# Kernel tuning notes

Hardware: AMD Instinct MI355X
Metric: run time of the kernel (lower is better)

Reference implementation:

```python
import jax, jax.numpy as jnp
import numpy as np
import math
from jax import lax

IMG = 800.0
STRIDES = (8, 16, 32)
SIZES = (100, 50, 25)
PAD = 100
ANCHOR_SIZES = (32., 64., 128., 256., 512.)
RATIOS = (0.5, 1.0, 2.0)
A = 15
PRE_NMS = 500
POST_NMS = 512
RPN_NMS_THR = 0.7
BOX_NMS_THR = 0.5
SCORE_THR = 0.05
DETS = 100
POOL = 7
SR = 2
CH = 256
NUM_CLASSES = 2
CLIP = math.log(1000.0 / 16)


def _grid_anchors():
    scales = np.array(ANCHOR_SIZES, np.float32)
    hr = np.sqrt(np.array(RATIOS, np.float32)); wr = 1.0 / hr
    ws = (wr[:, None] * scales[None]).reshape(-1)
    hs = (hr[:, None] * scales[None]).reshape(-1)
    base = np.stack([-ws, -hs, ws, hs], 1) / 2.0
    out = []
    for stride, s in zip(STRIDES, SIZES):
        sx = np.arange(s, dtype=np.float32) * stride
        yy, xx = np.meshgrid(sx, sx, indexing='ij')
        shifts = np.stack([xx, yy, xx, yy], -1).reshape(-1, 1, 4)
        out.append(jnp.asarray((shifts + base[None]).reshape(-1, 4)))
    return out


def conv2d(x, w, b, pad):
    y = lax.conv_general_dilated(x, w, (1, 1), pad, dimension_numbers=('NCHW', 'OIHW', 'NCHW'))
    return y + b[None, :, None, None]


def decode(deltas, boxes, weights):
    w = boxes[:, 2] - boxes[:, 0]; h = boxes[:, 3] - boxes[:, 1]
    cx = boxes[:, 0] + 0.5 * w; cy = boxes[:, 1] + 0.5 * h
    dx = deltas[:, 0] / weights[0]; dy = deltas[:, 1] / weights[1]
    dw = jnp.minimum(deltas[:, 2] / weights[2], CLIP)
    dh = jnp.minimum(deltas[:, 3] / weights[3], CLIP)
    pcx = dx * w + cx; pcy = dy * h + cy
    pw = jnp.exp(dw) * w; ph = jnp.exp(dh) * h
    return jnp.stack([pcx - 0.5 * pw, pcy - 0.5 * ph, pcx + 0.5 * pw, pcy + 0.5 * ph], 1)


def pairwise_iou(a, b):
    aa = (a[:, 2] - a[:, 0]) * (a[:, 3] - a[:, 1])
    ab = (b[:, 2] - b[:, 0]) * (b[:, 3] - b[:, 1])
    lt = jnp.maximum(a[:, None, :2], b[None, :, :2])
    rb = jnp.minimum(a[:, None, 2:], b[None, :, 2:])
    wh = jnp.maximum(rb - lt, 0.0)
    inter = wh[..., 0] * wh[..., 1]
    return inter / (aa[:, None] + ab[None, :] - inter + 1e-9)


def nms_keep(boxes, scores, thr):
    # greedy NMS, fixed-size boolean keep mask (jit-friendly)
    N = boxes.shape[0]
    order = jnp.argsort(-scores)
    iou = pairwise_iou(boxes[order], boxes[order])
    idx = jnp.arange(N)
    def body(i, keep):
        sup = keep[i] & (iou[i] > thr) & (idx > i)
        return keep & (~sup)
    keep = lax.fori_loop(0, N, body, jnp.ones((N,), bool))
    return jnp.zeros((N,), bool).at[order].set(keep)


def rpn_proposals(objs, dels, anchors):
    sb, ss, sl = [], [], []
    for lvl in range(3):
        s, i = lax.top_k(objs[lvl], PRE_NMS)
        b = decode(dels[lvl][i], anchors[lvl][i], (1., 1., 1., 1.))
        sb.append(jnp.clip(b, 0.0, IMG)); ss.append(s)
        sl.append(jnp.full((PRE_NMS,), float(lvl), jnp.float32))
    boxes = jnp.concatenate(sb); scores = jnp.concatenate(ss); lvl = jnp.concatenate(sl)
    valid = (boxes[:, 2] - boxes[:, 0] >= 1e-3) & (boxes[:, 3] - boxes[:, 1] >= 1e-3)
    scores = jnp.where(valid, scores, -1e9)
    # batched NMS across levels via coordinate offset trick
    keep = lax.stop_gradient(nms_keep(boxes + (lvl * (IMG + 16.0))[:, None], scores, RPN_NMS_THR))
    _, top = lax.top_k(jnp.where(keep, scores, -1e9), POST_NMS)
    return boxes[top]


def roi_align_image(flat, boxes):
    # flat: [3*PAD*PAD, CH] level-major padded pyramid, boxes: [N,4]
    sizes = jnp.asarray(SIZES, jnp.float32)
    strides = jnp.asarray(STRIDES, jnp.float32)
    def one(box):
        x1, y1, x2, y2 = box[0], box[1], box[2], box[3]
        area = jnp.maximum(x2 - x1, 0.0) * jnp.maximum(y2 - y1, 0.0)
        k = jnp.floor(4.0 + jnp.log2(jnp.sqrt(area) / 224.0 + 1e-6))
        lvl = jnp.clip(k, 3.0, 5.0).astype(jnp.int32) - 3
        sc = 1.0 / strides[lvl]; hw = sizes[lvl]
        rx1 = x1 * sc; ry1 = y1 * sc
        rw = jnp.maximum(x2 * sc - rx1, 1.0); rh = jnp.maximum(y2 * sc - ry1, 1.0)
        bw = rw / POOL; bh = rh / POOL
        g = jnp.arange(POOL, dtype=jnp.float32)
        sg = (jnp.arange(SR, dtype=jnp.float32) + 0.5) / SR
        ys = ry1 + (g[:, None] + sg[None, :]) * bh  # [7,2]
        xs = rx1 + (g[:, None] + sg[None, :]) * bw
        Y = jnp.broadcast_to(ys[:, None, :, None], (POOL, POOL, SR, SR)).reshape(-1)
        X = jnp.broadcast_to(xs[None, :, None, :], (POOL, POOL, SR, SR)).reshape(-1)
        Y = jnp.clip(Y, 0.0, hw - 1.0); X = jnp.clip(X, 0.0, hw - 1.0)
        y0 = jnp.floor(Y); x0 = jnp.floor(X)
        ly = Y - y0; lx = X - x0
        y0i = y0.astype(jnp.int32); x0i = x0.astype(jnp.int32)
        hi = (hw - 1.0).astype(jnp.int32)
        y1i = jnp.minimum(y0i + 1, hi); x1i = jnp.minimum(x0i + 1, hi)
        base = lvl * (PAD * PAD)
        ws = ((1 - ly) * (1 - lx), (1 - ly) * lx, ly * (1 - lx), ly * lx)
        ids = (base + y0i * PAD + x0i, base + y0i * PAD + x1i,
               base + y1i * PAD + x0i, base + y1i * PAD + x1i)
        acc = ws[0][:, None] * flat[ids[0]]
        for kk in range(1, 4):
            acc = acc + ws[kk][:, None] * flat[ids[kk]]
        out = acc.reshape(POOL, POOL, SR * SR, CH).mean(2)  # avg over 2x2 samples
        return jnp.transpose(out, (2, 0, 1))  # [CH,7,7]
    return jax.vmap(one)(boxes)


def postprocess(cls_logits, deltas, boxes):
    scores = jax.nn.softmax(cls_logits, -1)[:, 1]
    pb = jnp.clip(decode(deltas.reshape(-1, NUM_CLASSES, 4)[:, 1], boxes, (10., 10., 5., 5.)), 0.0, IMG)
    valid = (scores > SCORE_THR) & (pb[:, 2] - pb[:, 0] >= 1e-2) & (pb[:, 3] - pb[:, 1] >= 1e-2)
    s = jnp.where(valid, scores, -1e9)
    keep = lax.stop_gradient(nms_keep(pb, s, BOX_NMS_THR)) & valid
    s = jnp.where(keep, scores, 0.0)
    ts, ti = lax.top_k(s, DETS)
    ok = (ts > 0.0).astype(pb.dtype)
    return jnp.concatenate([pb[ti] * ok[:, None], ts[:, None], ok[:, None]], 1)  # [DETS,6]


def _forward(feat0, feat1, feat2, rpn_conv_w, rpn_conv_b, rpn_cls_w, rpn_cls_b,
             rpn_box_w, rpn_box_b, fc1_w, fc1_b, fc2_w, fc2_b, cls_w, cls_b, box_w, box_b):
    feats = (feat0, feat1, feat2)
    anchors = _grid_anchors()
    B = feat0.shape[0]
    objs, dels = [], []
    for f in feats:
        t = jax.nn.relu(conv2d(f, rpn_conv_w, rpn_conv_b, 'SAME'))
        o = conv2d(t, rpn_cls_w, rpn_cls_b, 'VALID')  # [B,A,H,W]
        d = conv2d(t, rpn_box_w, rpn_box_b, 'VALID')  # [B,4A,H,W]
        H, W = o.shape[2], o.shape[3]
        objs.append(o.transpose(0, 2, 3, 1).reshape(B, -1))
        dels.append(d.reshape(B, A, 4, H, W).transpose(0, 3, 4, 1, 2).reshape(B, -1, 4))
    props = jax.vmap(lambda o0, o1, o2, d0, d1, d2:
                     rpn_proposals((o0, o1, o2), (d0, d1, d2), anchors))(
        objs[0], objs[1], objs[2], dels[0], dels[1], dels[2])  # [B,POST_NMS,4]
    pyr = jnp.stack([jnp.pad(f, ((0, 0), (0, 0), (0, PAD - f.shape[2]), (0, PAD - f.shape[3])))
                     for f in feats], 1)  # [B,3,CH,PAD,PAD]
    flat = pyr.transpose(0, 1, 3, 4, 2).reshape(B, 3 * PAD * PAD, CH)
    roi = jax.vmap(roi_align_image)(flat, props)  # [B,N,CH,7,7]
    x = roi.reshape(B * POST_NMS, CH * POOL * POOL)
    x = jax.nn.relu(x @ fc1_w + fc1_b)
    x = jax.nn.relu(x @ fc2_w + fc2_b)
    cls = (x @ cls_w + cls_b).reshape(B, POST_NMS, NUM_CLASSES)
    dlt = (x @ box_w + box_b).reshape(B, POST_NMS, NUM_CLASSES * 4)
    return jax.vmap(postprocess)(cls, dlt, props)  # [B,DETS,6]


def setup_inputs():
    key = jax.random.key(0)
    ks = jax.random.split(key, 16)
    r = lambda k, shp, s=0.05: jax.random.normal(k, shp, jnp.float32) * s
    return {
        'feat0': r(ks[0], (2, CH, 100, 100), 1.0),
        'feat1': r(ks[1], (2, CH, 50, 50), 1.0),
        'feat2': r(ks[2], (2, CH, 25, 25), 1.0),
        'rpn_conv_w': r(ks[3], (CH, CH, 3, 3)),
        'rpn_conv_b': jnp.zeros((CH,), jnp.float32),
        'rpn_cls_w': r(ks[4], (A, CH, 1, 1)),
        'rpn_cls_b': jnp.zeros((A,), jnp.float32),
        'rpn_box_w': r(ks[5], (4 * A, CH, 1, 1)),
        'rpn_box_b': jnp.zeros((4 * A,), jnp.float32),
        'fc1_w': r(ks[6], (CH * POOL * POOL, 1024), 0.01),
        'fc1_b': jnp.zeros((1024,), jnp.float32),
        'fc2_w': r(ks[7], (1024, 1024), 0.01),
        'fc2_b': jnp.zeros((1024,), jnp.float32),
        'cls_w': r(ks[8], (1024, NUM_CLASSES), 0.01),
        'cls_b': jnp.zeros((NUM_CLASSES,), jnp.float32),
        'box_w': r(ks[9], (1024, NUM_CLASSES * 4), 0.01),
        'box_b': jnp.zeros((NUM_CLASSES * 4,), jnp.float32),
    }


def reference(feat0, feat1, feat2, rpn_conv_w, rpn_conv_b, rpn_cls_w, rpn_cls_b,
              rpn_box_w, rpn_box_b, fc1_w, fc1_b, fc2_w, fc2_b, cls_w, cls_b, box_w, box_b):
    return _forward(feat0, feat1, feat2, rpn_conv_w, rpn_conv_b, rpn_cls_w, rpn_cls_b,
                    rpn_box_w, rpn_box_b, fc1_w, fc1_b, fc2_w, fc2_b, cls_w, cls_b, box_w, box_b)
```

## Files before the change

### kernel.cpp

```cpp
#include <hip/hip_runtime.h>
#include <hip/hip_bf16.h>
#include <stdint.h>

#define IMGF 800.0f
#define CLIPF 4.135166556742356f

typedef __attribute__((ext_vector_type(8))) short bf16x8;
typedef __attribute__((ext_vector_type(4))) float f32x4;
typedef __attribute__((ext_vector_type(8))) unsigned short u16x8;
#define MFMA32 __builtin_amdgcn_mfma_f32_16x16x32_bf16

__device__ __forceinline__ uint32_t fkey(float x){
  uint32_t b = __float_as_uint(x);
  return (b & 0x80000000u) ? ~b : (b | 0x80000000u);
}

__device__ __forceinline__ float bf2f(unsigned short h){
  return __uint_as_float(((uint32_t)h)<<16);
}

__device__ __forceinline__ unsigned short f2bf(float x){
  __hip_bfloat16 hb = __float2bfloat16(x);
  return *reinterpret_cast<unsigned short*>(&hb);
}

__device__ __forceinline__ void split3(float x,
    unsigned short&h, unsigned short&m, unsigned short&l){
  h = f2bf(x);
  float r = x - bf2f(h);
  m = f2bf(r);
  float s = r - bf2f(m);
  l = f2bf(s);
}

__device__ __forceinline__ void split3x2(float x0, float x1,
    unsigned short&h0, unsigned short&h1, unsigned short&m0, unsigned short&m1,
    unsigned short&l0, unsigned short&l1){
  __hip_bfloat162 hb = __float22bfloat162_rn(make_float2(x0,x1));
  ushort2 hu = *reinterpret_cast<ushort2*>(&hb);
  float r0 = x0 - bf2f(hu.x), r1 = x1 - bf2f(hu.y);
  __hip_bfloat162 mb = __float22bfloat162_rn(make_float2(r0,r1));
  ushort2 mu = *reinterpret_cast<ushort2*>(&mb);
  float s0 = r0 - bf2f(mu.x), s1 = r1 - bf2f(mu.y);
  __hip_bfloat162 lb = __float22bfloat162_rn(make_float2(s0,s1));
  ushort2 lu = *reinterpret_cast<ushort2*>(&lb);
  h0=hu.x; h1=hu.y; m0=mu.x; m1=mu.y; l0=lu.x; l1=lu.y;
}

__device__ void bitonic_desc(unsigned long long* k, int n, int tid, int nthr){
  for (int kk=2; kk<=n; kk<<=1){
    for (int j=kk>>1; j>0; j>>=1){
      __syncthreads();
      for (int i=tid; i<n; i+=nthr){
        int ixj = i ^ j;
        if (ixj > i){
          unsigned long long a = k[i], b = k[ixj];
          bool up = ((i & kk) == 0);
          if ((a < b) == up){ k[i]=b; k[ixj]=a; }
        }
      }
    }
  }
  __syncthreads();
}

__global__ __launch_bounds__(256) void prep_all(
    const float* __restrict__ w, const float* __restrict__ wc,
    const float* __restrict__ wb,
    unsigned short* __restrict__ wBh, unsigned short* __restrict__ wBm,
    unsigned short* __restrict__ wBl, float* __restrict__ wrp2,
    uint32_t* __restrict__ zbuf){
  int bid = blockIdx.x;
  if (bid < 2304){
    int idx = bid*256 + threadIdx.x;
    int oc = idx & 255; int rest = idx >> 8;
    int ic = rest & 255; int d = rest >> 8;
    float v = w[((size_t)oc*256 + ic)*9 + d];
    unsigned short h,m,l; split3(v,h,m,l);
    wBh[idx]=h; wBm[idx]=m; wBl[idx]=l;
  } else if (bid < 2384){
    int idx = (bid-2304)*256 + threadIdx.x;
    if (idx < 4*256*20){
      int j = idx % 20; int rest = idx/20;
      int cc = rest & 255; int wv = rest >> 8;
      int o = wv + 4*j;
      float v = 0.f;
      if (j < 19 && o < 75) v = (o<15) ? wc[o*256+cc] : wb[(o-15)*256+cc];
      wrp2[idx] = v;
    }
  } else {
    int i = (bid-2384)*256 + threadIdx.x;
    if (i < 50696) zbuf[i] = 0u;
  }
}

__global__ __launch_bounds__(256) void conv_mfma(
    const float* __restrict__ featT,
    const unsigned short* __restrict__ wBh, const unsigned short* __restrict__ wBm,
    const unsigned short* __restrict__ wBl,
    const float* __restrict__ bias, float* __restrict__ tP){
  __shared__ unsigned short Ah[128*40], Amm[128*40], Al[128*40];
  __shared__ unsigned short Bh[64*40],  Bmm[64*40],  Bl[64*40];
  const int tid = threadIdx.x;
  const int bid = blockIdx.x;
  const int xcd = bid & 7, jb = bid >> 3;
  const int rt  = xcd*26 + (jb >> 2);
  const int bn  = (jb & 3) * 64;
  const int b = rt / 104;
  const int i = rt - b*104;
  int base, HW, W, posOff;
  if (i < 79)      { base = i*128;        HW = 10000; W = 100; posOff = 0; }
  else if (i < 99) { base = (i-79)*128;   HW = 2500;  W = 50;  posOff = 10000; }
  else             { base = (i-99)*128;   HW = 625;   W = 25;  posOff = 12500; }
  const int gRowBase = b*13125 + posOff;

  const int lane = tid & 63, wv = tid >> 6;
  const int wm = (wv>>1)*64, wn = (wv&1)*32;
  const int fr = lane & 15, fq = lane >> 4;

  const int arow = tid >> 1;
  const int ak   = (tid & 1) * 16;
  const int apos = base + arow;
  const bool av  = apos < HW;
  const int ay = apos / W, ax = apos - ay*W;
  const float* arowp = featT + (size_t)(gRowBase + apos)*256;
  const int bnl = tid & 63, bk0 = (tid >> 6) * 8;

  f32x4 acc[4][2];
  #pragma unroll
  for (int mi=0;mi<4;mi++)
    #pragma unroll
    for (int ni=0;ni<2;ni++) acc[mi][ni] = (f32x4){0.f,0.f,0.f,0.f};

  float va[16];
  u16x8 vbh, vbm, vbl;
  int dcur = -1, shift = 0; bool okf = false;

  auto loadA = [&](int step){
    const int kb = step*32;
    const int d  = kb >> 8;
    if (d != dcur){
      dcur = d;
      const int q3 = (d*11) >> 5;
      const int dy = q3 - 1, dx = d - 3*q3 - 1;
      shift = (dy*W + dx)*256;
      okf = av && (unsigned)(ay+dy) < (unsigned)W && (unsigned)(ax+dx) < (unsigned)W;
    }
    const int ic0 = (kb & 255) + ak;
    if (okf){
      #pragma unroll
      for (int c=0;c<4;c++){
        float4 f = *reinterpret_cast<const float4*>(arowp + shift + ic0 + c*4);
        va[c*4+0]=f.x; va[c*4+1]=f.y; va[c*4+2]=f.z; va[c*4+3]=f.w;
      }
    } else {
      #pragma unroll
      for (int c=0;c<16;c++) va[c]=0.f;
    }
  };
  auto loadB = [&](int step){
    const int kb = step*32;
    #pragma unroll
    for (int j=0;j<8;j++){
      size_t idx = (size_t)(kb + bk0 + j)*256 + bn + bnl;
      vbh[j] = wBh[idx]; vbm[j] = wBm[idx]; vbl[j] = wBl[idx];
    }
  };
  auto storeAB = [&](){
    u16x8 h[2], m[2], l[2];
    #pragma unroll
    for (int c=0;c<2;c++)
      #pragma unroll
      for (int p=0;p<4;p++){
        unsigned short h0,h1,m0,m1,l0,l1;
        split3x2(va[c*8+p*2], va[c*8+p*2+1], h0,h1,m0,m1,l0,l1);
        h[c][p*2]=h0; h[c][p*2+1]=h1;
        m[c][p*2]=m0; m[c][p*2+1]=m1;
        l[c][p*2]=l0; l[c][p*2+1]=l1;
      }
    const int ao = arow*40 + ak;
    *reinterpret_cast<u16x8*>(&Ah [ao])   = h[0];
    *reinterpret_cast<u16x8*>(&Ah [ao+8]) = h[1];
    *reinterpret_cast<u16x8*>(&Amm[ao])   = m[0];
    *reinterpret_cast<u16x8*>(&Amm[ao+8]) = m[1];
    *reinterpret_cast<u16x8*>(&Al [ao])   = l[0];
    *reinterpret_cast<u16x8*>(&Al [ao+8]) = l[1];
    const int bo = bnl*40 + bk0;
    *reinterpret_cast<u16x8*>(&Bh [bo]) = vbh;
    *reinterpret_cast<u16x8*>(&Bmm[bo]) = vbm;
    *reinterpret_cast<u16x8*>(&Bl [bo]) = vbl;
  };

  loadA(0); loadB(0);
  storeAB();
  __syncthreads();

  const int T = 72;
  for (int t=0; t<T; ++t){
    if (t+1 < T){ loadA(t+1); loadB(t+1); }
    bf16x8 aH[4], aM[4], aL[4];
    #pragma unroll
    for (int mi=0;mi<4;mi++){
      const int ro = (wm + mi*16 + fr)*40 + fq*8;
      aH[mi] = *reinterpret_cast<const bf16x8*>(&Ah [ro]);
      aM[mi] = *reinterpret_cast<const bf16x8*>(&Amm[ro]);
      aL[mi] = *reinterpret_cast<const bf16x8*>(&Al [ro]);
    }
    #pragma unroll
    for (int ni=0;ni<2;ni++){
      const int co = (wn + ni*16 + fr)*40 + fq*8;
      bf16x8 bH = *reinterpret_cast<const bf16x8*>(&Bh [co]);
      bf16x8 bM = *reinterpret_cast<const bf16x8*>(&Bmm[co]);
      bf16x8 bL = *reinterpret_cast<const bf16x8*>(&Bl [co]);
      #pragma unroll
      for (int mi=0;mi<4;mi++){
        f32x4 a = acc[mi][ni];
        a = MFMA32(aL[mi], bH, a, 0,0,0);
        a = MFMA32(aM[mi], bM, a, 0,0,0);
        a = MFMA32(aH[mi], bL, a, 0,0,0);
        a = MFMA32(aM[mi], bH, a, 0,0,0);
        a = MFMA32(aH[mi], bM, a, 0,0,0);
        a = MFMA32(aH[mi], bH, a, 0,0,0);
        acc[mi][ni] = a;
      }
    }
    if (t+1 < T){
      __syncthreads();
      storeAB();
      __syncthreads();
    }
  }

  #pragma unroll
  for (int mi=0;mi<4;mi++){
    #pragma unroll
    for (int ni=0;ni<2;ni++){
      const int col = bn + wn + ni*16 + fr;
      const float bz = bias[col];
      #pragma unroll
      for (int r=0;r<4;r++){
        const int pos = base + wm + mi*16 + fq*4 + r;
        if (pos < HW)
          tP[(size_t)(gRowBase+pos)*256 + col] = fmaxf(acc[mi][ni][r] + bz, 0.f);
      }
    }
  }
}

__global__ __launch_bounds__(256) void gemm_mfma(
    const float* __restrict__ Am, const float* __restrict__ Bm,
    float* __restrict__ part, int M, int N, int K, int KC){
  __shared__ unsigned short Ah[128*40], Amm[128*40], Al[128*40];
  __shared__ unsigned short Bh[64*40],  Bmm[64*40],  Bl[64*40];
  const int tid = threadIdx.x;
  const int bn = blockIdx.x*64, bm = blockIdx.y*128, kz = blockIdx.z;
  const int k0 = kz*KC;
  const int T = KC/32;

  const int lane = tid & 63, wv = tid >> 6;
  const int wm = (wv>>1)*64, wn = (wv&1)*32;
  const int fr = lane & 15, fq = lane >> 4;

  const int arow = tid >> 1;
  const int ak   = (tid & 1) * 16;
  const int bnl = tid & 63, bk0 = (tid >> 6) * 8;

  f32x4 acc[4][2];
  #pragma unroll
  for (int mi=0;mi<4;mi++)
    #pragma unroll
    for (int ni=0;ni<2;ni++) acc[mi][ni] = (f32x4){0.f,0.f,0.f,0.f};

  float va[16], vb[8];

  auto loadA = [&](int kb){
    const float* p = &Am[(size_t)(bm+arow)*K + kb + ak];
    #pragma unroll
    for (int c=0;c<4;c++){
      float4 f = *reinterpret_cast<const float4*>(p + c*4);
      va[c*4+0]=f.x; va[c*4+1]=f.y; va[c*4+2]=f.z; va[c*4+3]=f.w;
    }
  };
  auto loadB = [&](int kb){
    #pragma unroll
    for (int j=0;j<8;j++) vb[j] = Bm[(size_t)(kb + bk0 + j)*N + bn + bnl];
  };
  auto storeAB = [&](){
    u16x8 h[2], m[2], l[2];
    #pragma unroll
    for (int c=0;c<2;c++)
      #pragma unroll
      for (int p=0;p<4;p++){
        unsigned short h0,h1,m0,m1,l0,l1;
        split3x2(va[c*8+p*2], va[c*8+p*2+1], h0,h1,m0,m1,l0,l1);
        h[c][p*2]=h0; h[c][p*2+1]=h1;
        m[c][p*2]=m0; m[c][p*2+1]=m1;
        l[c][p*2]=l0; l[c][p*2+1]=l1;
      }
    const int ao = arow*40 + ak;
    *reinterpret_cast<u16x8*>(&Ah [ao])   = h[0];
    *reinterpret_cast<u16x8*>(&Ah [ao+8]) = h[1];
    *reinterpret_cast<u16x8*>(&Amm[ao])   = m[0];
    *reinterpret_cast<u16x8*>(&Amm[ao+8]) = m[1];
    *reinterpret_cast<u16x8*>(&Al [ao])   = l[0];
    *reinterpret_cast<u16x8*>(&Al [ao+8]) = l[1];
    u16x8 hb, mb, lb;
    #pragma unroll
    for (int p=0;p<4;p++){
      unsigned short h0,h1,m0,m1,l0,l1;
      split3x2(vb[p*2], vb[p*2+1], h0,h1,m0,m1,l0,l1);
      hb[p*2]=h0; hb[p*2+1]=h1; mb[p*2]=m0; mb[p*2+1]=m1; lb[p*2]=l0; lb[p*2+1]=l1;
    }
    const int bo = bnl*40 + bk0;
    *reinterpret_cast<u16x8*>(&Bh [bo]) = hb;
    *reinterpret_cast<u16x8*>(&Bmm[bo]) = mb;
    *reinterpret_cast<u16x8*>(&Bl [bo]) = lb;
  };

  loadA(k0); loadB(k0);
  storeAB();
  __syncthreads();

  for (int t=0; t<T; ++t){
    if (t+1 < T){ loadA(k0 + (t+1)*32); loadB(k0 + (t+1)*32); }
    bf16x8 aH[4], aM[4], aL[4];
    #pragma unroll
    for (int mi=0;mi<4;mi++){
      const int ro = (wm + mi*16 + fr)*40 + fq*8;
      aH[mi] = *reinterpret_cast<const bf16x8*>(&Ah [ro]);
      aM[mi] = *reinterpret_cast<const bf16x8*>(&Amm[ro]);
      aL[mi] = *reinterpret_cast<const bf16x8*>(&Al [ro]);
    }
    #pragma unroll
    for (int ni=0;ni<2;ni++){
      const int co = (wn + ni*16 + fr)*40 + fq*8;
      bf16x8 bH = *reinterpret_cast<const bf16x8*>(&Bh [co]);
      bf16x8 bM = *reinterpret_cast<const bf16x8*>(&Bmm[co]);
      bf16x8 bL = *reinterpret_cast<const bf16x8*>(&Bl [co]);
      #pragma unroll
      for (int mi=0;mi<4;mi++){
        f32x4 a = acc[mi][ni];
        a = MFMA32(aL[mi], bH, a, 0,0,0);
        a = MFMA32(aM[mi], bM, a, 0,0,0);
        a = MFMA32(aH[mi], bL, a, 0,0,0);
        a = MFMA32(aM[mi], bH, a, 0,0,0);
        a = MFMA32(aH[mi], bM, a, 0,0,0);
        a = MFMA32(aH[mi], bH, a, 0,0,0);
        acc[mi][ni] = a;
      }
    }
    if (t+1 < T){
      __syncthreads();
      storeAB();
      __syncthreads();
    }
  }

  float* pz = part + (size_t)kz*M*N;
  #pragma unroll
  for (int mi=0;mi<4;mi++){
    #pragma unroll
    for (int ni=0;ni<2;ni++){
      const int col = bn + wn + ni*16 + fr;
      #pragma unroll
      for (int r=0;r<4;r++){
        const int row = bm + wm + mi*16 + fq*4 + r;
        pz[(size_t)row*N + col] = acc[mi][ni][r];
      }
    }
  }
}

__global__ __launch_bounds__(256) void rpn_heads_all(
    const float* __restrict__ tP, const float* __restrict__ wrp2,
    const float* __restrict__ bc, const float* __restrict__ bb,
    float* __restrict__ objs, float* __restrict__ dels){
  int bx = blockIdx.x;
  int HW, posOff, lvlOff, gx;
  if (bx < 157)      { gx = bx;     HW = 10000; posOff = 0;     lvlOff = 0; }
  else if (bx < 197) { gx = bx-157; HW = 2500;  posOff = 10000; lvlOff = 150000; }
  else               { gx = bx-197; HW = 625;   posOff = 12500; lvlOff = 187500; }
  int b = blockIdx.y;
  int p0 = gx*64;
  int lane = threadIdx.x & 63;
  int wv = __builtin_amdgcn_readfirstlane(threadIdx.x >> 6);
  __shared__ float sh[64][129];
  float acc[19];
  #pragma unroll
  for (int j=0;j<19;j++) acc[j]=0.f;
  const float* tb = tP + (size_t)(b*13125 + posOff)*256;
  for (int half=0; half<2; ++half){
    __syncthreads();
    for (int idx=threadIdx.x; idx<64*128; idx+=256){
      int px = idx>>7, c = idx&127;
      int p = p0+px;
      sh[px][c] = (p<HW) ? tb[(size_t)p*256 + half*128 + c] : 0.f;
    }
    __syncthreads();
    for (int c=0;c<128;c++){
      float v = sh[lane][c];
      int cc = half*128 + c;
      const float* wr = wrp2 + ((size_t)wv*256 + cc)*20;
      #pragma unroll
      for (int j=0;j<19;j++){
        int o = wv + 4*j;
        if (o < 75) acc[j] += v*wr[j];
      }
    }
  }
  int p = p0 + lane;
  if (p < HW){
    #pragma unroll
    for (int j=0;j<19;j++){
      int o = wv + 4*j;
      if (o < 75){
        if (o < 15){
          objs[(size_t)b*196875 + lvlOff + (size_t)p*15 + o] = acc[j] + bc[o];
        } else {
          int q = o-15;
          dels[((size_t)b*196875 + lvlOff + (size_t)p*15 + (q>>2))*4 + (q&3)] = acc[j] + bb[q];
        }
      }
    }
  }
}

__global__ __launch_bounds__(256) void feat_transpose_all(
    const float* __restrict__ f0, const float* __restrict__ f1,
    const float* __restrict__ f2, float* __restrict__ ft){
  __shared__ float tile[32][33];
  int bx = blockIdx.x;
  const float* f; int HW, posOff, gx;
  if (bx < 313)      { f = f0; gx = bx;     HW = 10000; posOff = 0; }
  else if (bx < 392) { f = f1; gx = bx-313; HW = 2500;  posOff = 10000; }
  else               { f = f2; gx = bx-392; HW = 625;   posOff = 12500; }
  int b = blockIdx.z;
  int p0 = gx*32, c0 = blockIdx.y*32;
  int tx = threadIdx.x & 31, ty = threadIdx.x >> 5;
  #pragma unroll
  for (int i=0;i<4;i++){
    int c = c0 + ty + i*8;
    int p = p0 + tx;
    tile[ty+i*8][tx] = (p<HW) ? f[((size_t)b*256 + c)*HW + p] : 0.f;
  }
  __syncthreads();
  #pragma unroll
  for (int i=0;i<4;i++){
    int p = p0 + ty + i*8;
    int c = c0 + tx;
    if (p < HW) ft[((size_t)b*13125 + posOff + p)*256 + c] = tile[tx][ty+i*8];
  }
}

__device__ __forceinline__ void tk_params(int pl, int& b, int& lvl, int& N, int& off){
  b = pl/3; lvl = pl - b*3;
  const int Ns[3]   = {150000,37500,9375};
  const int Offs[3] = {0,150000,187500};
  N = Ns[lvl]; off = Offs[lvl];
}

__device__ void suffix_select(uint32_t* s, int NB, int K, int tid,
                              int* outB, int* outK){
  for (int step=1; step<NB; step<<=1){
    uint32_t v[4]; int c=0;
    for (int i=tid;i<NB;i+=1024){ v[c++] = s[i] + ((i+step<NB)?s[i+step]:0u); }
    __syncthreads();
    c=0;
    for (int i=tid;i<NB;i+=1024) s[i]=v[c++];
    __syncthreads();
  }
  for (int i=tid;i<NB;i+=1024){
    int sufi = (int)s[i];
    int sufn = (i+1<NB)?(int)s[i+1]:0;
    if (sufi >= K && sufn < K){ *outB = i; *outK = K - sufn; }
  }
  __syncthreads();
}

__global__ __launch_bounds__(1024) void tk_hist1(
    const float* __restrict__ objs, uint32_t* __restrict__ gh1){
  __shared__ uint32_t h[4096];
  int pl = blockIdx.y, b, lvl, N, off;
  tk_params(pl,b,lvl,N,off);
  const float* sc = objs + (size_t)b*196875 + off;
  int tid = threadIdx.x;
  for (int i=tid;i<4096;i+=1024) h[i]=0u;
  __syncthreads();
  int cs = (N+7)>>3;
  int s0 = blockIdx.x*cs, s1 = s0+cs; if (s1>N) s1=N;
  for (int i=s0+tid;i<s1;i+=1024) atomicAdd(&h[fkey(sc[i])>>20],1u);
  __syncthreads();
  uint32_t* g = gh1 + pl*4096;
  for (int i=tid;i<4096;i+=1024) if(h[i]) atomicAdd(&g[i],h[i]);
}

__global__ __launch_bounds__(1024) void tk_hist2(
    const float* __restrict__ objs, const uint32_t* __restrict__ gh1,
    uint32_t* __restrict__ gh2){
  __shared__ uint32_t s[4096];
  __shared__ int sB, sK;
  int pl = blockIdx.y, b, lvl, N, off;
  tk_params(pl,b,lvl,N,off);
  const float* sc = objs + (size_t)b*196875 + off;
  int tid = threadIdx.x;
  for (int i=tid;i<4096;i+=1024) s[i]=gh1[pl*4096+i];
  __syncthreads();
  suffix_select(s,4096,500,tid,&sB,&sK);
  const uint32_t B1 = (uint32_t)sB;
  __syncthreads();
  for (int i=tid;i<4096;i+=1024) s[i]=0u;
  __syncthreads();
  int cs = (N+7)>>3;
  int s0 = blockIdx.x*cs, s1 = s0+cs; if (s1>N) s1=N;
  for (int i=s0+tid;i<s1;i+=1024){
    uint32_t u = fkey(sc[i]);
    if ((u>>20)==B1) atomicAdd(&s[(u>>8)&0xFFFu],1u);
  }
  __syncthreads();
  uint32_t* g = gh2 + pl*4096;
  for (int i=tid;i<4096;i+=1024) if(s[i]) atomicAdd(&g[i],s[i]);
}

__global__ __launch_bounds__(1024) void tk_hist3(
    const float* __restrict__ objs, const uint32_t* __restrict__ gh1,
    const uint32_t* __restrict__ gh2, uint32_t* __restrict__ gh3){
  __shared__ uint32_t s[4096];
  __shared__ int sB, sK;
  int pl = blockIdx.y, b, lvl, N, off;
  tk_params(pl,b,lvl,N,off);
  const float* sc = objs + (size_t)b*196875 + off;
  int tid = threadIdx.x;
  for (int i=tid;i<4096;i+=1024) s[i]=gh1[pl*4096+i];
  __syncthreads();
  suffix_select(s,4096,500,tid,&sB,&sK);
  const uint32_t B1 = (uint32_t)sB; const int k1 = sK;
  __syncthreads();
  for (int i=tid;i<4096;i+=1024) s[i]=gh2[pl*4096+i];
  __syncthreads();
  suffix_select(s,4096,k1,tid,&sB,&sK);
  const uint32_t B2 = (uint32_t)sB;
  const uint32_t pref24 = (B1<<12)|B2;
  __syncthreads();
  for (int i=tid;i<256;i+=1024) s[i]=0u;
  __syncthreads();
  int cs = (N+7)>>3;
  int s0 = blockIdx.x*cs, s1 = s0+cs; if (s1>N) s1=N;
  for (int i=s0+tid;i<s1;i+=1024){
    uint32_t u = fkey(sc[i]);
    if ((u>>8)==pref24) atomicAdd(&s[u & 0xFFu],1u);
  }
  __syncthreads();
  uint32_t* g = gh3 + pl*256;
  for (int i=tid;i<256;i+=1024) if(s[i]) atomicAdd(&g[i],s[i]);
}

__global__ __launch_bounds__(1024) void tk_compact(
    const float* __restrict__ objs, const uint32_t* __restrict__ gh1,
    const uint32_t* __restrict__ gh2, const uint32_t* __restrict__ gh3,
    int* __restrict__ candCnt, unsigned long long* __restrict__ cand){
  __shared__ uint32_t s[4096];
  __shared__ int sB, sK;
  int pl = blockIdx.y, b, lvl, N, off;
  tk_params(pl,b,lvl,N,off);
  const float* sc = objs + (size_t)b*196875 + off;
  int tid = threadIdx.x;
  for (int i=tid;i<4096;i+=1024) s[i]=gh1[pl*4096+i];
  __syncthreads();
  suffix_select(s,4096,500,tid,&sB,&sK);
  const uint32_t B1 = (uint32_t)sB; const int k1 = sK;
  __syncthreads();
  for (int i=tid;i<4096;i+=1024) s[i]=gh2[pl*4096+i];
  __syncthreads();
  suffix_select(s,4096,k1,tid,&sB,&sK);
  const uint32_t B2 = (uint32_t)sB; const int k2 = sK;
  __syncthreads();
  for (int i=tid;i<256;i+=1024) s[i]=gh3[pl*256+i];
  __syncthreads();
  suffix_select(s,256,k2,tid,&sB,&sK);
  const uint32_t B3 = (uint32_t)sB;
  const uint32_t T = (B1<<20)|(B2<<8)|B3;
  int cs = (N+7)>>3;
  int s0 = blockIdx.x*cs, s1 = s0+cs; if (s1>N) s1=N;
  unsigned long long* cp = cand + (size_t)pl*4096;
  for (int i=s0+tid;i<s1;i+=1024){
    uint32_t u = fkey(sc[i]);
    if (u >= T){
      int pos = atomicAdd(&candCnt[pl], 1);
      if (pos < 4096)
        cp[pos] = ((unsigned long long)u<<32) | (uint32_t)(~(uint32_t)i);
    }
  }
}

__global__ __launch_bounds__(1024) void tk_sortdecode(
    const float* __restrict__ objs, const float* __restrict__ dels,
    const int* __restrict__ candCnt, const unsigned long long* __restrict__ cand,
    float* __restrict__ lvl_boxes, float* __restrict__ lvl_scores){
  const int lvl = blockIdx.x, b = blockIdx.y;
  const int pl = b*3 + lvl;
  const int Offs[3] = {0,150000,187500};
  const int Wl[3]   = {100,50,25};
  const float strid[3] = {8.f,16.f,32.f};
  const float* sc = objs + (size_t)b*196875 + Offs[lvl];
  __shared__ unsigned long long keys[4096];
  int tid = threadIdx.x;
  int m = candCnt[pl]; if (m > 4096) m = 4096;
  int n = 512; while (n < m) n <<= 1;
  const unsigned long long* cp = cand + (size_t)pl*4096;
  for (int i=tid;i<n;i+=1024) keys[i] = (i<m) ? cp[i] : 0ull;
  __syncthreads();
  bitonic_desc(keys, n, tid, 1024);
  if (tid < 500){
    unsigned long long key = keys[tid];
    uint32_t idx = ~(uint32_t)(key & 0xFFFFFFFFull);
    float score = sc[idx];
    int p = idx/15, a = idx - p*15;
    int W = Wl[lvl];
    int hh = p / W, ww = p - hh*W;
    int r5 = a/5, s5 = a - r5*5;
    const float ratios[3] = {0.5f,1.0f,2.0f};
    const float scales[5] = {32.f,64.f,128.f,256.f,512.f};
    float hr = sqrtf(ratios[r5]); float wr = 1.0f/hr;
    float wsz = wr*scales[s5], hsz = hr*scales[s5];
    float sx = (float)ww*strid[lvl], sy = (float)hh*strid[lvl];
    float ax1 = sx - 0.5f*wsz, ay1 = sy - 0.5f*hsz;
    float ax2 = sx + 0.5f*wsz, ay2 = sy + 0.5f*hsz;
    const float* dl = dels + ((size_t)b*196875 + Offs[lvl] + idx)*4;
    float bw = ax2-ax1, bh = ay2-ay1;
    float cx = ax1 + 0.5f*bw, cy = ay1 + 0.5f*bh;
    float dx = dl[0], dy = dl[1];
    float dw = fminf(dl[2], CLIPF), dh = fminf(dl[3], CLIPF);
    float pcx = dx*bw + cx, pcy = dy*bh + cy;
    float pw = expf(dw)*bw, ph = expf(dh)*bh;
    float x1 = fminf(fmaxf(pcx - 0.5f*pw, 0.f), IMGF);
    float y1 = fminf(fmaxf(pcy - 0.5f*ph, 0.f), IMGF);
    float x2 = fminf(fmaxf(pcx + 0.5f*pw, 0.f), IMGF);
    float y2 = fminf(fmaxf(pcy + 0.5f*ph, 0.f), IMGF);
    int oidx = b*1500 + lvl*500 + tid;
    lvl_boxes[oidx*4+0]=x1; lvl_boxes[oidx*4+1]=y1;
    lvl_boxes[oidx*4+2]=x2; lvl_boxes[oidx*4+3]=y2;
    bool valid = (x2-x1 >= 1e-3f) && (y2-y1 >= 1e-3f);
    lvl_scores[oidx] = valid ? score : -1e9f;
  }
}

__global__ __launch_bounds__(1024) void nms_sort(
    const float* __restrict__ lvl_boxes, const float* __restrict__ lvl_scores,
    float* __restrict__ snb, int* __restrict__ sorder){
  int b = blockIdx.x, tid = threadIdx.x;
  __shared__ unsigned long long keys[2048];
  const float* ls = lvl_scores + (size_t)b*1500;
  const float* lb = lvl_boxes + (size_t)b*1500*4;
  for (int i=tid;i<2048;i+=1024)
    keys[i] = (i<1500) ? (((unsigned long long)fkey(ls[i])<<32)|(uint32_t)(~(uint32_t)i)) : 0ull;
  __syncthreads();
  bitonic_desc(keys, 2048, tid, 1024);
  for (int r=tid;r<1536;r+=1024){
    if (r < 1500){
      int idx = (int)(~(uint32_t)keys[r]);
      sorder[(size_t)b*1536 + r] = idx;
      float offv = (float)(idx/500) * (IMGF + 16.0f);
      float* pp = snb + ((size_t)b*1536 + r)*4;
      pp[0]=lb[idx*4+0]+offv; pp[1]=lb[idx*4+1]+offv;
      pp[2]=lb[idx*4+2]+offv; pp[3]=lb[idx*4+3]+offv;
    } else {
      sorder[(size_t)b*1536 + r] = 0;
      float* pp = snb + ((size_t)b*1536 + r)*4;
      pp[0]=pp[1]=pp[2]=pp[3]=0.f;
    }
  }
}

__global__ __launch_bounds__(256) void nms_mask(
    const float* __restrict__ snb, unsigned long long* __restrict__ masks){
  int b = blockIdx.y;
  int i0 = blockIdx.x*64;
  __shared__ float sbx[1536][4];
  for (int t=threadIdx.x; t<1536*4; t+=256)
    sbx[t>>2][t&3] = snb[(size_t)b*1536*4 + t];
  __syncthreads();
  int il = threadIdx.x >> 2;
  int wq = threadIdx.x & 3;
  int i = i0 + il;
  float ax1=sbx[i][0], ay1=sbx[i][1], ax2=sbx[i][2], ay2=sbx[i][3];
  float aa=(ax2-ax1)*(ay2-ay1);
  #pragma unroll
  for (int wofs=0; wofs<6; ++wofs){
    int w = wq*6 + wofs;
    unsigned long long m = 0ull;
    if (i < 1500){
      for (int jj=0; jj<64; ++jj){
        int j = w*64 + jj;
        if (j > i && j < 1500){
          float bx1=sbx[j][0],by1=sbx[j][1],bx2=sbx[j][2],by2=sbx[j][3];
          float ab=(bx2-bx1)*(by2-by1);
          float lx=fmaxf(ax1,bx1), ly=fmaxf(ay1,by1);
          float rx=fminf(ax2,bx2), ry=fminf(ay2,by2);
          float iw=fmaxf(rx-lx,0.f), ih=fmaxf(ry-ly,0.f);
          float inter=iw*ih;
          if (inter/(aa+ab-inter+1e-9f) > 0.7f) m |= (1ull<<jj);
        }
      }
    }
    masks[((size_t)b*1536 + i)*24 + w] = m;
  }
}

__global__ __launch_bounds__(1024) void nms_scan_final(
    const unsigned long long* __restrict__ masks, const int* __restrict__ sorder,
    const float* __restrict__ lvl_boxes, const float* __restrict__ lvl_scores,
    float* __restrict__ props){
  int b = blockIdx.x, tid = threadIdx.x;
  __shared__ unsigned long long cm[128][24];
  __shared__ volatile unsigned long long keepw[24];
  __shared__ unsigned char korig[1536];
  __shared__ unsigned long long keys[2048];
  if (tid < 24) keepw[tid] = (tid==23) ? ((1ull<<28)-1ull) : ~0ull;
  for (int c=0; c<12; ++c){
    __syncthreads();
    for (int t=tid; t<128*24; t+=1024)
      cm[t/24][t%24] = masks[((size_t)b*1536 + c*128)*24 + t];
    __syncthreads();
    if (tid < 24){
      int lim = (c==11) ? 84 : 128;
      for (int il=0; il<lim; ++il){
        int i = c*128 + il;
        unsigned long long kw = keepw[i>>6];
        if ((kw>>(i&63)) & 1ull) keepw[tid] &= ~cm[il][tid];
      }
    }
  }
  __syncthreads();
  for (int r=tid; r<1500; r+=1024){
    unsigned long long kw = keepw[r>>6];
    korig[sorder[(size_t)b*1536 + r]] = (unsigned char)((kw>>(r&63)) & 1ull);
  }
  __syncthreads();
  const float* ls = lvl_scores + (size_t)b*1500;
  const float* lb = lvl_boxes + (size_t)b*1500*4;
  for (int i=tid;i<2048;i+=1024){
    if (i<1500){
      float s = korig[i] ? ls[i] : -1e9f;
      keys[i] = ((unsigned long long)fkey(s)<<32)|(uint32_t)(~(uint32_t)i);
    } else keys[i]=0ull;
  }
  __syncthreads();
  bitonic_desc(keys, 2048, tid, 1024);
  for (int j=tid;j<512;j+=1024){
    int idx = (int)(~(uint32_t)keys[j]);
    float* pp = props + ((size_t)b*512 + j)*4;
    pp[0]=lb[idx*4+0]; pp[1]=lb[idx*4+1]; pp[2]=lb[idx*4+2]; pp[3]=lb[idx*4+3];
  }
}

__global__ __launch_bounds__(256) void roi_align(
    const float* __restrict__ featT, const float* __restrict__ props,
    float* __restrict__ roiX){
  int blk = blockIdx.x;
  int b = blk >> 9, n = blk & 511;
  const float* box = props + ((size_t)b*512 + n)*4;
  float x1=box[0], y1=box[1], x2=box[2], y2=box[3];
  float area = fmaxf(x2-x1,0.f)*fmaxf(y2-y1,0.f);
  float kf = floorf(4.0f + log2f(sqrtf(area)/224.0f + 1e-6f));
  kf = fminf(fmaxf(kf, 3.f), 5.f);
  int lvl = (int)kf - 3;
  const int Wl[3] = {100,50,25};
  const int posOff[3] = {0,10000,12500};
  const float strid[3] = {8.f,16.f,32.f};
  float scl = 1.0f/strid[lvl];
  float hw = (float)Wl[lvl];
  float rx1 = x1*scl, ry1 = y1*scl;
  float rw = fmaxf(x2*scl - rx1, 1.0f), rh = fmaxf(y2*scl - ry1, 1.0f);
  float bw = rw/7.0f, bh = rh/7.0f;
  __shared__ int sIdx[196][4];
  __shared__ float sW[196][4];
  int t = threadIdx.x;
  if (t < 196){
    int bin = t>>2, s = t&3;
    int py = bin/7, px = bin - py*7;
    int sy = s>>1, sx = s&1;
    float sgy = ((float)sy + 0.5f)*0.5f, sgx = ((float)sx + 0.5f)*0.5f;
    float Y = ry1 + ((float)py + sgy)*bh;
    float X = rx1 + ((float)px + sgx)*bw;
    Y = fminf(fmaxf(Y,0.f), hw-1.0f);
    X = fminf(fmaxf(X,0.f), hw-1.0f);
    float y0 = floorf(Y), x0 = floorf(X);
    float ly = Y-y0, lx = X-x0;
    int y0i=(int)y0, x0i=(int)x0;
    int hi = Wl[lvl]-1;
    int y1i = (y0i+1<hi)?(y0i+1):hi;
    int x1i = (x0i+1<hi)?(x0i+1):hi;
    int W = Wl[lvl];
    int base = b*13125 + posOff[lvl];
    sIdx[t][0] = (base + y0i*W + x0i)*256;
    sIdx[t][1] = (base + y0i*W + x1i)*256;
    sIdx[t][2] = (base + y1i*W + x0i)*256;
    sIdx[t][3] = (base + y1i*W + x1i)*256;
    sW[t][0]=(1.f-ly)*(1.f-lx); sW[t][1]=(1.f-ly)*lx;
    sW[t][2]=ly*(1.f-lx);       sW[t][3]=ly*lx;
  }
  __syncthreads();
  int c = t;
  float* orow = roiX + ((size_t)b*512 + n)*12544 + (size_t)c*49;
  for (int bin=0;bin<49;bin++){
    float acc = 0.f;
    #pragma unroll
    for (int s=0;s<4;s++){
      int tt = bin*4+s;
      acc += sW[tt][0]*featT[sIdx[tt][0]+c] + sW[tt][1]*featT[sIdx[tt][1]+c]
           + sW[tt][2]*featT[sIdx[tt][2]+c] + sW[tt][3]*featT[sIdx[tt][3]+c];
    }
    orow[bin] = acc*0.25f;
  }
}

__global__ __launch_bounds__(256) void reduce_splitk(
    const float* __restrict__ part, const float* __restrict__ bias,
    float* __restrict__ out, int MN, int Nmask, int relu){
  int i4 = (blockIdx.x*256 + threadIdx.x)*4;
  if (i4 < MN){
    float4 s0 = *reinterpret_cast<const float4*>(&part[i4]);
    float4 s1 = *reinterpret_cast<const float4*>(&part[(size_t)MN + i4]);
    float4 s2 = *reinterpret_cast<const float4*>(&part[(size_t)2*MN + i4]);
    float4 s3 = *reinterpret_cast<const float4*>(&part[(size_t)3*MN + i4]);
    float4 bb = *reinterpret_cast<const float4*>(&bias[i4 & Nmask]);
    float4 r;
    r.x = s0.x+s1.x+s2.x+s3.x+bb.x;
    r.y = s0.y+s1.y+s2.y+s3.y+bb.y;
    r.z = s0.z+s1.z+s2.z+s3.z+bb.z;
    r.w = s0.w+s1.w+s2.w+s3.w+bb.w;
    if (relu){ r.x=fmaxf(r.x,0.f); r.y=fmaxf(r.y,0.f); r.z=fmaxf(r.z,0.f); r.w=fmaxf(r.w,0.f); }
    *reinterpret_cast<float4*>(&out[i4]) = r;
  }
}

__global__ __launch_bounds__(256) void fc_heads(
    const float* __restrict__ x,
    const float* __restrict__ wcls, const float* __restrict__ bcls,
    const float* __restrict__ wbox, const float* __restrict__ bbox,
    float* __restrict__ cls, float* __restrict__ box){
  int row = blockIdx.x, tid = threadIdx.x;
  __shared__ float xs[1024];
  *reinterpret_cast<float4*>(&xs[tid*4]) =
      *reinterpret_cast<const float4*>(&x[(size_t)row*1024 + tid*4]);
  __syncthreads();
  int w = tid >> 6, lane = tid & 63;
  for (int o=w; o<10; o+=4){
    float p = 0.f;
    if (o < 2){
      for (int k=lane;k<1024;k+=64) p += xs[k]*wcls[(size_t)k*2 + o];
    } else {
      int q = o-2;
      for (int k=lane;k<1024;k+=64) p += xs[k]*wbox[(size_t)k*8 + q];
    }
    #pragma unroll
    for (int off=32; off>0; off>>=1) p += __shfl_down(p, off);
    if (lane==0){
      if (o<2) cls[(size_t)row*2 + o] = p + bcls[o];
      else     box[(size_t)row*8 + (o-2)] = p + bbox[o-2];
    }
  }
}

__global__ __launch_bounds__(1024) void postprocess_kernel(
    const float* __restrict__ cls, const float* __restrict__ boxd,
    const float* __restrict__ props, float* __restrict__ out){
  int b = blockIdx.x, tid = threadIdx.x;
  __shared__ float pb[512][4];
  __shared__ float sraw[512];
  __shared__ float s2a[512];
  __shared__ unsigned long long keys[512];
  __shared__ unsigned short order_[512];
  __shared__ unsigned char kval[512];
  __shared__ unsigned char korig[512];
  __shared__ unsigned long long pm[512][8];
  __shared__ volatile unsigned long long kw2[8];
  if (tid < 8) kw2[tid] = ~0ull;
  if (tid < 512){
    int r = b*512 + tid;
    float c0 = cls[(size_t)r*2+0], c1 = cls[(size_t)r*2+1];
    float mx = fmaxf(c0,c1);
    float e0 = expf(c0-mx), e1 = expf(c1-mx);
    float s = e1/(e0+e1);
    const float* pr = props + (size_t)r*4;
    float x1=pr[0], y1=pr[1], x2=pr[2], y2=pr[3];
    float w = x2-x1, h = y2-y1;
    float cx = x1 + 0.5f*w, cy = y1 + 0.5f*h;
    const float* dl = boxd + (size_t)r*8 + 4;
    float dx = dl[0]/10.f, dy = dl[1]/10.f;
    float dw = fminf(dl[2]/5.f, CLIPF), dh = fminf(dl[3]/5.f, CLIPF);
    float pcx = dx*w + cx, pcy = dy*h + cy;
    float pw = expf(dw)*w, ph = expf(dh)*h;
    float bx1 = fminf(fmaxf(pcx-0.5f*pw,0.f), IMGF);
    float by1 = fminf(fmaxf(pcy-0.5f*ph,0.f), IMGF);
    float bx2 = fminf(fmaxf(pcx+0.5f*pw,0.f), IMGF);
    float by2 = fminf(fmaxf(pcy+0.5f*ph,0.f), IMGF);
    pb[tid][0]=bx1; pb[tid][1]=by1; pb[tid][2]=bx2; pb[tid][3]=by2;
    bool valid = (s > 0.05f) && (bx2-bx1 >= 1e-2f) && (by2-by1 >= 1e-2f);
    sraw[tid]=s; kval[tid] = valid ? 1 : 0;
    float sm = valid ? s : -1e9f;
    keys[tid] = ((unsigned long long)fkey(sm)<<32) | (uint32_t)(~(uint32_t)tid);
  }
  __syncthreads();
  bitonic_desc(keys, 512, tid, 1024);
  if (tid < 512) order_[tid] = (unsigned short)(~(uint32_t)keys[tid]);
  __syncthreads();
  {
    int r = tid >> 1;
    int oi = order_[r];
    float ax1=pb[oi][0],ay1=pb[oi][1],ax2=pb[oi][2],ay2=pb[oi][3];
    float aa=(ax2-ax1)*(ay2-ay1);
    #pragma unroll
    for (int wo=0; wo<4; ++wo){
      int w = (tid&1)*4 + wo;
      unsigned long long m = 0ull;
      for (int jj=0;jj<64;jj++){
        int j = w*64 + jj;
        if (j > r){
          int oj = order_[j];
          float bx1=pb[oj][0],by1=pb[oj][1],bx2=pb[oj][2],by2=pb[oj][3];
          float ab=(bx2-bx1)*(by2-by1);
          float lx=fmaxf(ax1,bx1), ly=fmaxf(ay1,by1);
          float rx=fminf(ax2,bx2), ry=fminf(ay2,by2);
          float iw=fmaxf(rx-lx,0.f), ih=fmaxf(ry-ly,0.f);
          float inter=iw*ih;
          if (inter/(aa+ab-inter+1e-9f) > 0.5f) m |= (1ull<<jj);
        }
      }
      pm[r][w] = m;
    }
  }
  __syncthreads();
  if (tid < 8){
    for (int i=0;i<512;i++){
      unsigned long long kwv = kw2[i>>6];
      if ((kwv>>(i&63)) & 1ull) kw2[tid] &= ~pm[i][tid];
    }
  }
  __syncthreads();
  if (tid < 512){
    unsigned long long kwv = kw2[tid>>6];
    korig[order_[tid]] = (unsigned char)((kwv>>(tid&63)) & 1ull);
  }
  __syncthreads();
  if (tid < 512){
    float s2 = (korig[tid] && kval[tid]) ? sraw[tid] : 0.f;
    s2a[tid] = s2;
    keys[tid] = ((unsigned long long)fkey(s2)<<32) | (uint32_t)(~(uint32_t)tid);
  }
  __syncthreads();
  bitonic_desc(keys, 512, tid, 1024);
  if (tid < 100){
    uint32_t idx = ~(uint32_t)keys[tid];
    float ts = s2a[idx];
    float ok = (ts > 0.f) ? 1.f : 0.f;
    float* op = out + ((size_t)b*100 + tid)*6;
    op[0]=pb[idx][0]*ok; op[1]=pb[idx][1]*ok;
    op[2]=pb[idx][2]*ok; op[3]=pb[idx][3]*ok;
    op[4]=ts; op[5]=ok;
  }
}

extern "C" void kernel_launch(void* const* d_in, const int* in_sizes, int n_in,
                              void* d_out, int out_size, void* d_ws, size_t ws_size,
                              hipStream_t stream){
  (void)in_sizes; (void)n_in; (void)out_size; (void)ws_size;
  const float* feat0 = (const float*)d_in[0];
  const float* feat1 = (const float*)d_in[1];
  const float* feat2 = (const float*)d_in[2];
  const float* rpn_conv_w = (const float*)d_in[3];
  const float* rpn_conv_b = (const float*)d_in[4];
  const float* rpn_cls_w  = (const float*)d_in[5];
  const float* rpn_cls_b  = (const float*)d_in[6];
  const float* rpn_box_w  = (const float*)d_in[7];
  const float* rpn_box_b  = (const float*)d_in[8];
  const float* fc1_w = (const float*)d_in[9];
  const float* fc1_b = (const float*)d_in[10];
  const float* fc2_w = (const float*)d_in[11];
  const float* fc2_b = (const float*)d_in[12];
  const float* cls_w = (const float*)d_in[13];
  const float* cls_b = (const float*)d_in[14];
  const float* box_w = (const float*)d_in[15];
  const float* box_b = (const float*)d_in[16];

  float* ws = (float*)d_ws;
  float* featT = ws;
  float* fc1o  = ws;
  float* fc2o  = ws + 1048576;
  float* clsb  = ws + 2097152;
  float* boxb  = ws + 2099200;
  float* parts = ws + 2107392;
  float* props = ws + 6720000;
  float* roiX  = ws + 6724096;
  float* tP    = roiX;
  float* objs       = roiX + 6720000;
  float* dels       = roiX + 7113750;
  float* lvl_boxes  = roiX + 8688750;
  float* lvl_scores = roiX + 8700750;
  float* nms_snb    = roiX + 8703750;
  int*   nms_order  = (int*)(roiX + 8716038);
  unsigned long long* nms_masks = (unsigned long long*)(roiX + 8719110);
  float* wrp2  = roiX + 8866568;
  unsigned short* wBh = (unsigned short*)(roiX + 8887048);
  unsigned short* wBm = (unsigned short*)(roiX + 9181960);
  unsigned short* wBl = (unsigned short*)(roiX + 9476872);
  uint32_t* gh1 = (uint32_t*)(roiX + 9771784);
  uint32_t* gh2 = (uint32_t*)(roiX + 9796360);
  uint32_t* gh3 = (uint32_t*)(roiX + 9820936);
  int*      candCnt = (int*)(roiX + 9822472);
  unsigned long long* cand = (unsigned long long*)(roiX + 9822480);

  prep_all<<<2583, 256, 0, stream>>>(rpn_conv_w, rpn_cls_w, rpn_box_w,
                                     wBh, wBm, wBl, wrp2, gh1);
  feat_transpose_all<<<dim3(412,8,2), 256, 0, stream>>>(feat0, feat1, feat2, featT);
  conv_mfma<<<832, 256, 0, stream>>>(featT, wBh, wBm, wBl, rpn_conv_b, tP);
  rpn_heads_all<<<dim3(207,2), 256, 0, stream>>>(tP, wrp2, rpn_cls_b, rpn_box_b, objs, dels);
  tk_hist1<<<dim3(8,6), 1024, 0, stream>>>(objs, gh1);
  tk_hist2<<<dim3(8,6), 1024, 0, stream>>>(objs, gh1, gh2);
  tk_hist3<<<dim3(8,6), 1024, 0, stream>>>(objs, gh1, gh2, gh3);
  tk_compact<<<dim3(8,6), 1024, 0, stream>>>(objs, gh1, gh2, gh3, candCnt, cand);
  tk_sortdecode<<<dim3(3,2), 1024, 0, stream>>>(objs, dels, candCnt, cand, lvl_boxes, lvl_scores);
  nms_sort<<<2, 1024, 0, stream>>>(lvl_boxes, lvl_scores, nms_snb, nms_order);
  nms_mask<<<dim3(24,2), 256, 0, stream>>>(nms_snb, nms_masks);
  nms_scan_final<<<2, 1024, 0, stream>>>(nms_masks, nms_order, lvl_boxes, lvl_scores, props);
  roi_align<<<1024, 256, 0, stream>>>(featT, props, roiX);
  gemm_mfma<<<dim3(16,8,4), 256, 0, stream>>>(roiX, fc1_w, parts, 1024, 1024, 12544, 3136);
  reduce_splitk<<<1024, 256, 0, stream>>>(parts, fc1_b, fc1o, 1024*1024, 1023, 1);
  gemm_mfma<<<dim3(16,8,4), 256, 0, stream>>>(fc1o, fc2_w, parts, 1024, 1024, 1024, 256);
  reduce_splitk<<<1024, 256, 0, stream>>>(parts, fc2_b, fc2o, 1024*1024, 1023, 1);
  fc_heads<<<1024, 256, 0, stream>>>(fc2o, cls_w, cls_b, box_w, box_b, clsb, boxb);
  postprocess_kernel<<<2, 1024, 0, stream>>>(clsb, boxb, props, (float*)d_out);
}
```

Baseline: 1.426 ms.

## Fuse pipeline stages to cut kernel launches across RPN, top-k, NMS and FC

Several stages are merged to reduce the number of launches and global round-trips. Weight prep and the feature transpose become one kernel, and the conv weight split into bf16 parts now happens inside the conv instead of in prep. The four top-k stages become one single-block-per-plane kernel, and the three NMS stages become one kernel. The fc1 split-K reduction plus bias and ReLU is folded into the fc2 GEMM's A-load, and fc2 drops split-K. The costs are less parallelism (6 blocks for top-k, 128 blocks for fc2) and repeated weight splitting inside the conv.

After: 1.983 ms (median of 2 runs). +39.1%, slower.

```diff
diff --git a/kernel.cpp b/kernel.cpp
--- a/kernel.cpp
+++ b/kernel.cpp
@@ -17,20 +17,6 @@
 
 __device__ __forceinline__ float bf2f(unsigned short h){
   return __uint_as_float(((uint32_t)h)<<16);
-}
-
-__device__ __forceinline__ unsigned short f2bf(float x){
-  __hip_bfloat16 hb = __float2bfloat16(x);
-  return *reinterpret_cast<unsigned short*>(&hb);
-}
-
-__device__ __forceinline__ void split3(float x,
-    unsigned short&h, unsigned short&m, unsigned short&l){
-  h = f2bf(x);
-  float r = x - bf2f(h);
-  m = f2bf(r);
-  float s = r - bf2f(m);
-  l = f2bf(s);
 }
 
 __device__ __forceinline__ void split3x2(float x0, float x1,
@@ -64,40 +50,64 @@
   __syncthreads();
 }
 
-__global__ __launch_bounds__(256) void prep_all(
+__global__ __launch_bounds__(256) void prep_tr(
     const float* __restrict__ w, const float* __restrict__ wc,
-    const float* __restrict__ wb,
-    unsigned short* __restrict__ wBh, unsigned short* __restrict__ wBm,
-    unsigned short* __restrict__ wBl, float* __restrict__ wrp2,
-    uint32_t* __restrict__ zbuf){
+    const float* __restrict__ wb, float* __restrict__ wB,
+    float* __restrict__ wrp2, uint32_t* __restrict__ gh1,
+    const float* __restrict__ f0, const float* __restrict__ f1,
+    const float* __restrict__ f2, float* __restrict__ ft){
   int bid = blockIdx.x;
   if (bid < 2304){
     int idx = bid*256 + threadIdx.x;
     int oc = idx & 255; int rest = idx >> 8;
     int ic = rest & 255; int d = rest >> 8;
-    float v = w[((size_t)oc*256 + ic)*9 + d];
-    unsigned short h,m,l; split3(v,h,m,l);
-    wBh[idx]=h; wBm[idx]=m; wBl[idx]=l;
-  } else if (bid < 2384){
+    wB[idx] = w[((size_t)oc*256 + ic)*9 + d];
+    return;
+  }
+  if (bid < 2384){
     int idx = (bid-2304)*256 + threadIdx.x;
-    if (idx < 4*256*20){
-      int j = idx % 20; int rest = idx/20;
-      int cc = rest & 255; int wv = rest >> 8;
-      int o = wv + 4*j;
-      float v = 0.f;
-      if (j < 19 && o < 75) v = (o<15) ? wc[o*256+cc] : wb[(o-15)*256+cc];
-      wrp2[idx] = v;
-    }
-  } else {
+    int j = idx % 20; int rest = idx/20;
+    int cc = rest & 255; int wv = rest >> 8;
+    int o = wv + 4*j;
+    float v = 0.f;
+    if (j < 19 && o < 75) v = (o<15) ? wc[o*256+cc] : wb[(o-15)*256+cc];
+    wrp2[idx] = v;
+    return;
+  }
+  if (bid < 2480){
     int i = (bid-2384)*256 + threadIdx.x;
-    if (i < 50696) zbuf[i] = 0u;
+    gh1[i] = 0u;
+    return;
+  }
+  __shared__ float tile[32][33];
+  int bt = bid - 2480;
+  int bx = bt % 412;
+  int rest = bt / 412;
+  int cy = rest & 7;
+  int b = rest >> 3;
+  const float* f; int HW, posOff, gx;
+  if (bx < 313)      { f = f0; gx = bx;     HW = 10000; posOff = 0; }
+  else if (bx < 392) { f = f1; gx = bx-313; HW = 2500;  posOff = 10000; }
+  else               { f = f2; gx = bx-392; HW = 625;   posOff = 12500; }
+  int p0 = gx*32, c0 = cy*32;
+  int tx = threadIdx.x & 31, ty = threadIdx.x >> 5;
+  #pragma unroll
+  for (int i=0;i<4;i++){
+    int c = c0 + ty + i*8;
+    int p = p0 + tx;
+    tile[ty+i*8][tx] = (p<HW) ? f[((size_t)b*256 + c)*HW + p] : 0.f;
+  }
+  __syncthreads();
+  #pragma unroll
+  for (int i=0;i<4;i++){
+    int p = p0 + ty + i*8;
+    int c = c0 + tx;
+    if (p < HW) ft[((size_t)b*13125 + posOff + p)*256 + c] = tile[tx][ty+i*8];
   }
 }
 
 __global__ __launch_bounds__(256) void conv_mfma(
-    const float* __restrict__ featT,
-    const unsigned short* __restrict__ wBh, const unsigned short* __restrict__ wBm,
-    const unsigned short* __restrict__ wBl,
+    const float* __restrict__ featT, const float* __restrict__ wB,
     const float* __restrict__ bias, float* __restrict__ tP){
   __shared__ unsigned short Ah[128*40], Amm[128*40], Al[128*40];
   __shared__ unsigned short Bh[64*40],  Bmm[64*40],  Bl[64*40];
@@ -132,8 +142,7 @@
     #pragma unroll
     for (int ni=0;ni<2;ni++) acc[mi][ni] = (f32x4){0.f,0.f,0.f,0.f};
 
-  float va[16];
-  u16x8 vbh, vbm, vbl;
+  float va[16], vb[8];
   int dcur = -1, shift = 0; bool okf = false;
 
   auto loadA = [&](int step){
@@ -161,10 +170,7 @@
   auto loadB = [&](int step){
     const int kb = step*32;
     #pragma unroll
-    for (int j=0;j<8;j++){
-      size_t idx = (size_t)(kb + bk0 + j)*256 + bn + bnl;
-      vbh[j] = wBh[idx]; vbm[j] = wBm[idx]; vbl[j] = wBl[idx];
-    }
+    for (int j=0;j<8;j++) vb[j] = wB[(size_t)(kb + bk0 + j)*256 + bn + bnl];
   };
   auto storeAB = [&](){
     u16x8 h[2], m[2], l[2];
@@ -185,10 +191,17 @@
     *reinterpret_cast<u16x8*>(&Amm[ao+8]) = m[1];
     *reinterpret_cast<u16x8*>(&Al [ao])   = l[0];
     *reinterpret_cast<u16x8*>(&Al [ao+8]) = l[1];
+    u16x8 hb, mb, lb;
+    #pragma unroll
+    for (int p=0;p<4;p++){
+      unsigned short h0,h1,m0,m1,l0,l1;
+      split3x2(vb[p*2], vb[p*2+1], h0,h1,m0,m1,l0,l1);
+      hb[p*2]=h0; hb[p*2+1]=h1; mb[p*2]=m0; mb[p*2+1]=m1; lb[p*2]=l0; lb[p*2+1]=l1;
+    }
     const int bo = bnl*40 + bk0;
-    *reinterpret_cast<u16x8*>(&Bh [bo]) = vbh;
-    *reinterpret_cast<u16x8*>(&Bmm[bo]) = vbm;
-    *reinterpret_cast<u16x8*>(&Bl [bo]) = vbl;
+    *reinterpret_cast<u16x8*>(&Bh [bo]) = hb;
+    *reinterpret_cast<u16x8*>(&Bmm[bo]) = mb;
+    *reinterpret_cast<u16x8*>(&Bl [bo]) = lb;
   };
 
   loadA(0); loadB(0);
@@ -366,6 +379,138 @@
       for (int r=0;r<4;r++){
         const int row = bm + wm + mi*16 + fq*4 + r;
         pz[(size_t)row*N + col] = acc[mi][ni][r];
+      }
+    }
+  }
+}
+
+__global__ __launch_bounds__(256) void gemm_fc2(
+    const float* __restrict__ parts, const float* __restrict__ bias1,
+    const float* __restrict__ Bm, const float* __restrict__ bias2,
+    float* __restrict__ out){
+  __shared__ unsigned short Ah[128*40], Amm[128*40], Al[128*40];
+  __shared__ unsigned short Bh[64*40],  Bmm[64*40],  Bl[64*40];
+  const int tid = threadIdx.x;
+  const int bn = blockIdx.x*64, bm = blockIdx.y*128;
+  const int MN = 1024*1024;
+  const int T = 32;
+
+  const int lane = tid & 63, wv = tid >> 6;
+  const int wm = (wv>>1)*64, wn = (wv&1)*32;
+  const int fr = lane & 15, fq = lane >> 4;
+
+  const int arow = tid >> 1;
+  const int ak   = (tid & 1) * 16;
+  const int bnl = tid & 63, bk0 = (tid >> 6) * 8;
+
+  f32x4 acc[4][2];
+  #pragma unroll
+  for (int mi=0;mi<4;mi++)
+    #pragma unroll
+    for (int ni=0;ni<2;ni++) acc[mi][ni] = (f32x4){0.f,0.f,0.f,0.f};
+
+  float va[16], vb[8];
+
+  auto loadA = [&](int kb){
+    const float* p = parts + (size_t)(bm+arow)*1024 + kb + ak;
+    #pragma unroll
+    for (int c=0;c<4;c++){
+      float4 f0 = *reinterpret_cast<const float4*>(p + c*4);
+      float4 f1 = *reinterpret_cast<const float4*>(p + MN + c*4);
+      float4 f2 = *reinterpret_cast<const float4*>(p + 2*MN + c*4);
+      float4 f3 = *reinterpret_cast<const float4*>(p + 3*MN + c*4);
+      float4 bb = *reinterpret_cast<const float4*>(&bias1[kb + ak + c*4]);
+      va[c*4+0]=fmaxf(f0.x+f1.x+f2.x+f3.x+bb.x, 0.f);
+      va[c*4+1]=fmaxf(f0.y+f1.y+f2.y+f3.y+bb.y, 0.f);
+      va[c*4+2]=fmaxf(f0.z+f1.z+f2.z+f3.z+bb.z, 0.f);
+      va[c*4+3]=fmaxf(f0.w+f1.w+f2.w+f3.w+bb.w, 0.f);
+    }
+  };
+  auto loadB = [&](int kb){
+    #pragma unroll
+    for (int j=0;j<8;j++) vb[j] = Bm[(size_t)(kb + bk0 + j)*1024 + bn + bnl];
+  };
+  auto storeAB = [&](){
+    u16x8 h[2], m[2], l[2];
+    #pragma unroll
+    for (int c=0;c<2;c++)
+      #pragma unroll
+      for (int p=0;p<4;p++){
+        unsigned short h0,h1,m0,m1,l0,l1;
+        split3x2(va[c*8+p*2], va[c*8+p*2+1], h0,h1,m0,m1,l0,l1);
+        h[c][p*2]=h0; h[c][p*2+1]=h1;
+        m[c][p*2]=m0; m[c][p*2+1]=m1;
+        l[c][p*2]=l0; l[c][p*2+1]=l1;
+      }
+    const int ao = arow*40 + ak;
+    *reinterpret_cast<u16x8*>(&Ah [ao])   = h[0];
+    *reinterpret_cast<u16x8*>(&Ah [ao+8]) = h[1];
+    *reinterpret_cast<u16x8*>(&Amm[ao])   = m[0];
+    *reinterpret_cast<u16x8*>(&Amm[ao+8]) = m[1];
+    *reinterpret_cast<u16x8*>(&Al [ao])   = l[0];
+    *reinterpret_cast<u16x8*>(&Al [ao+8]) = l[1];
+    u16x8 hb, mb, lb;
+    #pragma unroll
+    for (int p=0;p<4;p++){
+      unsigned short h0,h1,m0,m1,l0,l1;
+      split3x2(vb[p*2], vb[p*2+1], h0,h1,m0,m1,l0,l1);
+      hb[p*2]=h0; hb[p*2+1]=h1; mb[p*2]=m0; mb[p*2+1]=m1; lb[p*2]=l0; lb[p*2+1]=l1;
+    }
+    const int bo = bnl*40 + bk0;
+    *reinterpret_cast<u16x8*>(&Bh [bo]) = hb;
+    *reinterpret_cast<u16x8*>(&Bmm[bo]) = mb;
+    *reinterpret_cast<u16x8*>(&Bl [bo]) = lb;
+  };
+
+  loadA(0); loadB(0);
+  storeAB();
+  __syncthreads();
+
+  for (int t=0; t<T; ++t){
+    if (t+1 < T){ loadA((t+1)*32); loadB((t+1)*32); }
+    bf16x8 aH[4], aM[4], aL[4];
+    #pragma unroll
+    for (int mi=0;mi<4;mi++){
+      const int ro = (wm + mi*16 + fr)*40 + fq*8;
+      aH[mi] = *reinterpret_cast<const bf16x8*>(&Ah [ro]);
+      aM[mi] = *reinterpret_cast<const bf16x8*>(&Amm[ro]);
+      aL[mi] = *reinterpret_cast<const bf16x8*>(&Al [ro]);
+    }
+    #pragma unroll
+    for (int ni=0;ni<2;ni++){
+      const int co = (wn + ni*16 + fr)*40 + fq*8;
+      bf16x8 bH = *reinterpret_cast<const bf16x8*>(&Bh [co]);
+      bf16x8 bM = *reinterpret_cast<const bf16x8*>(&Bmm[co]);
+      bf16x8 bL = *reinterpret_cast<const bf16x8*>(&Bl [co]);
+      #pragma unroll
+      for (int mi=0;mi<4;mi++){
+        f32x4 a = acc[mi][ni];
+        a = MFMA32(aL[mi], bH, a, 0,0,0);
+        a = MFMA32(aM[mi], bM, a, 0,0,0);
+        a = MFMA32(aH[mi], bL, a, 0,0,0);
+        a = MFMA32(aM[mi], bH, a, 0,0,0);
+        a = MFMA32(aH[mi], bM, a, 0,0,0);
+        a = MFMA32(aH[mi], bH, a, 0,0,0);
+        acc[mi][ni] = a;
+      }
+    }
+    if (t+1 < T){
+      __syncthreads();
+      storeAB();
+      __syncthreads();
+    }
+  }
+
+  #pragma unroll
+  for (int mi=0;mi<4;mi++){
+    #pragma unroll
+    for (int ni=0;ni<2;ni++){
+      const int col = bn + wn + ni*16 + fr;
+      const float bz = bias2[col];
+      #pragma unroll
+      for (int r=0;r<4;r++){
+        const int row = bm + wm + mi*16 + fq*4 + r;
+        out[(size_t)row*1024 + col] = fmaxf(acc[mi][ni][r] + bz, 0.f);
       }
     }
   }
@@ -425,33 +570,6 @@
   }
 }
 
-__global__ __launch_bounds__(256) void feat_transpose_all(
-    const float* __restrict__ f0, const float* __restrict__ f1,
-    const float* __restrict__ f2, float* __restrict__ ft){
-  __shared__ float tile[32][33];
-  int bx = blockIdx.x;
-  const float* f; int HW, posOff, gx;
-  if (bx < 313)      { f = f0; gx = bx;     HW = 10000; posOff = 0; }
-  else if (bx < 392) { f = f1; gx = bx-313; HW = 2500;  posOff = 10000; }
-  else               { f = f2; gx = bx-392; HW = 625;   posOff = 12500; }
-  int b = blockIdx.z;
-  int p0 = gx*32, c0 = blockIdx.y*32;
-  int tx = threadIdx.x & 31, ty = threadIdx.x >> 5;
-  #pragma unroll
-  for (int i=0;i<4;i++){
-    int c = c0 + ty + i*8;
-    int p = p0 + tx;
-    tile[ty+i*8][tx] = (p<HW) ? f[((size_t)b*256 + c)*HW + p] : 0.f;
-  }
-  __syncthreads();
-  #pragma unroll
-  for (int i=0;i<4;i++){
-    int p = p0 + ty + i*8;
-    int c = c0 + tx;
-    if (p < HW) ft[((size_t)b*13125 + posOff + p)*256 + c] = tile[tx][ty+i*8];
-  }
-}
-
 __device__ __forceinline__ void tk_params(int pl, int& b, int& lvl, int& N, int& off){
   b = pl/3; lvl = pl - b*3;
   const int Ns[3]   = {150000,37500,9375};
@@ -494,126 +612,65 @@
   for (int i=tid;i<4096;i+=1024) if(h[i]) atomicAdd(&g[i],h[i]);
 }
 
-__global__ __launch_bounds__(1024) void tk_hist2(
-    const float* __restrict__ objs, const uint32_t* __restrict__ gh1,
-    uint32_t* __restrict__ gh2){
+__global__ __launch_bounds__(1024) void tk_rest(
+    const float* __restrict__ objs, const float* __restrict__ dels,
+    const uint32_t* __restrict__ gh1,
+    float* __restrict__ lvl_boxes, float* __restrict__ lvl_scores){
   __shared__ uint32_t s[4096];
-  __shared__ int sB, sK;
-  int pl = blockIdx.y, b, lvl, N, off;
+  __shared__ int sB, sK, cnt;
+  __shared__ unsigned long long cand[4096];
+  const int pl = blockIdx.x;
+  int b, lvl, N, off;
   tk_params(pl,b,lvl,N,off);
   const float* sc = objs + (size_t)b*196875 + off;
-  int tid = threadIdx.x;
+  const int tid = threadIdx.x;
   for (int i=tid;i<4096;i+=1024) s[i]=gh1[pl*4096+i];
   __syncthreads();
   suffix_select(s,4096,500,tid,&sB,&sK);
-  const uint32_t B1 = (uint32_t)sB;
+  const uint32_t B1 = (uint32_t)sB; const int k1 = sK;
   __syncthreads();
   for (int i=tid;i<4096;i+=1024) s[i]=0u;
   __syncthreads();
-  int cs = (N+7)>>3;
-  int s0 = blockIdx.x*cs, s1 = s0+cs; if (s1>N) s1=N;
-  for (int i=s0+tid;i<s1;i+=1024){
+  for (int i=tid;i<N;i+=1024){
     uint32_t u = fkey(sc[i]);
     if ((u>>20)==B1) atomicAdd(&s[(u>>8)&0xFFFu],1u);
   }
   __syncthreads();
-  uint32_t* g = gh2 + pl*4096;
-  for (int i=tid;i<4096;i+=1024) if(s[i]) atomicAdd(&g[i],s[i]);
-}
-
-__global__ __launch_bounds__(1024) void tk_hist3(
-    const float* __restrict__ objs, const uint32_t* __restrict__ gh1,
-    const uint32_t* __restrict__ gh2, uint32_t* __restrict__ gh3){
-  __shared__ uint32_t s[4096];
-  __shared__ int sB, sK;
-  int pl = blockIdx.y, b, lvl, N, off;
-  tk_params(pl,b,lvl,N,off);
-  const float* sc = objs + (size_t)b*196875 + off;
-  int tid = threadIdx.x;
-  for (int i=tid;i<4096;i+=1024) s[i]=gh1[pl*4096+i];
-  __syncthreads();
-  suffix_select(s,4096,500,tid,&sB,&sK);
-  const uint32_t B1 = (uint32_t)sB; const int k1 = sK;
-  __syncthreads();
-  for (int i=tid;i<4096;i+=1024) s[i]=gh2[pl*4096+i];
-  __syncthreads();
   suffix_select(s,4096,k1,tid,&sB,&sK);
-  const uint32_t B2 = (uint32_t)sB;
+  const uint32_t B2 = (uint32_t)sB; const int k2 = sK;
   const uint32_t pref24 = (B1<<12)|B2;
   __syncthreads();
   for (int i=tid;i<256;i+=1024) s[i]=0u;
   __syncthreads();
-  int cs = (N+7)>>3;
-  int s0 = blockIdx.x*cs, s1 = s0+cs; if (s1>N) s1=N;
-  for (int i=s0+tid;i<s1;i+=1024){
+  for (int i=tid;i<N;i+=1024){
     uint32_t u = fkey(sc[i]);
     if ((u>>8)==pref24) atomicAdd(&s[u & 0xFFu],1u);
   }
-  __syncthreads();
-  uint32_t* g = gh3 + pl*256;
-  for (int i=tid;i<256;i+=1024) if(s[i]) atomicAdd(&g[i],s[i]);
-}
-
-__global__ __launch_bounds__(1024) void tk_compact(
-    const float* __restrict__ objs, const uint32_t* __restrict__ gh1,
-    const uint32_t* __restrict__ gh2, const uint32_t* __restrict__ gh3,
-    int* __restrict__ candCnt, unsigned long long* __restrict__ cand){
-  __shared__ uint32_t s[4096];
-  __shared__ int sB, sK;
-  int pl = blockIdx.y, b, lvl, N, off;
-  tk_params(pl,b,lvl,N,off);
-  const float* sc = objs + (size_t)b*196875 + off;
-  int tid = threadIdx.x;
-  for (int i=tid;i<4096;i+=1024) s[i]=gh1[pl*4096+i];
-  __syncthreads();
-  suffix_select(s,4096,500,tid,&sB,&sK);
-  const uint32_t B1 = (uint32_t)sB; const int k1 = sK;
-  __syncthreads();
-  for (int i=tid;i<4096;i+=1024) s[i]=gh2[pl*4096+i];
-  __syncthreads();
-  suffix_select(s,4096,k1,tid,&sB,&sK);
-  const uint32_t B2 = (uint32_t)sB; const int k2 = sK;
-  __syncthreads();
-  for (int i=tid;i<256;i+=1024) s[i]=gh3[pl*256+i];
   __syncthreads();
   suffix_select(s,256,k2,tid,&sB,&sK);
   const uint32_t B3 = (uint32_t)sB;
   const uint32_t T = (B1<<20)|(B2<<8)|B3;
-  int cs = (N+7)>>3;
-  int s0 = blockIdx.x*cs, s1 = s0+cs; if (s1>N) s1=N;
-  unsigned long long* cp = cand + (size_t)pl*4096;
-  for (int i=s0+tid;i<s1;i+=1024){
+  if (tid==0) cnt=0;
+  __syncthreads();
+  for (int i=tid;i<N;i+=1024){
     uint32_t u = fkey(sc[i]);
     if (u >= T){
-      int pos = atomicAdd(&candCnt[pl], 1);
-      if (pos < 4096)
-        cp[pos] = ((unsigned long long)u<<32) | (uint32_t)(~(uint32_t)i);
-    }
-  }
-}
-
-__global__ __launch_bounds__(1024) void tk_sortdecode(
-    const float* __restrict__ objs, const float* __restrict__ dels,
-    const int* __restrict__ candCnt, const unsigned long long* __restrict__ cand,
-    float* __restrict__ lvl_boxes, float* __restrict__ lvl_scores){
-  const int lvl = blockIdx.x, b = blockIdx.y;
-  const int pl = b*3 + lvl;
-  const int Offs[3] = {0,150000,187500};
-  const int Wl[3]   = {100,50,25};
-  const float strid[3] = {8.f,16.f,32.f};
-  const float* sc = objs + (size_t)b*196875 + Offs[lvl];
-  __shared__ unsigned long long keys[4096];
-  int tid = threadIdx.x;
-  int m = candCnt[pl]; if (m > 4096) m = 4096;
-  int n = 512; while (n < m) n <<= 1;
-  const unsigned long long* cp = cand + (size_t)pl*4096;
-  for (int i=tid;i<n;i+=1024) keys[i] = (i<m) ? cp[i] : 0ull;
-  __syncthreads();
-  bitonic_desc(keys, n, tid, 1024);
+      int p = atomicAdd(&cnt,1);
+      if (p < 4096) cand[p] = ((unsigned long long)u<<32) | (uint32_t)(~(uint32_t)i);
+    }
+  }
+  __syncthreads();
+  int m = cnt; if (m>4096) m=4096;
+  int n = 512; while (n<m) n<<=1;
+  for (int i=tid;i<n;i+=1024) if (i>=m) cand[i]=0ull;
+  __syncthreads();
+  bitonic_desc(cand, n, tid, 1024);
   if (tid < 500){
-    unsigned long long key = keys[tid];
+    unsigned long long key = cand[tid];
     uint32_t idx = ~(uint32_t)(key & 0xFFFFFFFFull);
     float score = sc[idx];
+    const int Wl[3]   = {100,50,25};
+    const float strid[3] = {8.f,16.f,32.f};
     int p = idx/15, a = idx - p*15;
     int W = Wl[lvl];
     int hh = p / W, ww = p - hh*W;
@@ -625,7 +682,7 @@
     float sx = (float)ww*strid[lvl], sy = (float)hh*strid[lvl];
     float ax1 = sx - 0.5f*wsz, ay1 = sy - 0.5f*hsz;
     float ax2 = sx + 0.5f*wsz, ay2 = sy + 0.5f*hsz;
-    const float* dl = dels + ((size_t)b*196875 + Offs[lvl] + idx)*4;
+    const float* dl = dels + ((size_t)b*196875 + off + idx)*4;
     float bw = ax2-ax1, bh = ay2-ay1;
     float cx = ax1 + 0.5f*bw, cy = ay1 + 0.5f*bh;
     float dx = dl[0], dy = dl[1];
@@ -644,11 +701,15 @@
   }
 }
 
-__global__ __launch_bounds__(1024) void nms_sort(
+__global__ __launch_bounds__(1024) void nms_all(
     const float* __restrict__ lvl_boxes, const float* __restrict__ lvl_scores,
-    float* __restrict__ snb, int* __restrict__ sorder){
+    unsigned long long* __restrict__ masks, float* __restrict__ props){
   int b = blockIdx.x, tid = threadIdx.x;
   __shared__ unsigned long long keys[2048];
+  __shared__ __align__(16) float sbx[6144];
+  __shared__ unsigned short order_[1536];
+  __shared__ unsigned char korig[1536];
+  __shared__ volatile unsigned long long keepw[24];
   const float* ls = lvl_scores + (size_t)b*1500;
   const float* lb = lvl_boxes + (size_t)b*1500*4;
   for (int i=tid;i<2048;i+=1024)
@@ -658,90 +719,63 @@
   for (int r=tid;r<1536;r+=1024){
     if (r < 1500){
       int idx = (int)(~(uint32_t)keys[r]);
-      sorder[(size_t)b*1536 + r] = idx;
+      order_[r] = (unsigned short)idx;
       float offv = (float)(idx/500) * (IMGF + 16.0f);
-      float* pp = snb + ((size_t)b*1536 + r)*4;
-      pp[0]=lb[idx*4+0]+offv; pp[1]=lb[idx*4+1]+offv;
-      pp[2]=lb[idx*4+2]+offv; pp[3]=lb[idx*4+3]+offv;
+      sbx[r*4+0]=lb[idx*4+0]+offv; sbx[r*4+1]=lb[idx*4+1]+offv;
+      sbx[r*4+2]=lb[idx*4+2]+offv; sbx[r*4+3]=lb[idx*4+3]+offv;
     } else {
-      sorder[(size_t)b*1536 + r] = 0;
-      float* pp = snb + ((size_t)b*1536 + r)*4;
-      pp[0]=pp[1]=pp[2]=pp[3]=0.f;
-    }
-  }
-}
-
-__global__ __launch_bounds__(256) void nms_mask(
-    const float* __restrict__ snb, unsigned long long* __restrict__ masks){
-  int b = blockIdx.y;
-  int i0 = blockIdx.x*64;
-  __shared__ float sbx[1536][4];
-  for (int t=threadIdx.x; t<1536*4; t+=256)
-    sbx[t>>2][t&3] = snb[(size_t)b*1536*4 + t];
-  __syncthreads();
-  int il = threadIdx.x >> 2;
-  int wq = threadIdx.x & 3;
-  int i = i0 + il;
-  float ax1=sbx[i][0], ay1=sbx[i][1], ax2=sbx[i][2], ay2=sbx[i][3];
-  float aa=(ax2-ax1)*(ay2-ay1);
-  #pragma unroll
-  for (int wofs=0; wofs<6; ++wofs){
-    int w = wq*6 + wofs;
+      order_[r] = 0;
+      sbx[r*4+0]=sbx[r*4+1]=sbx[r*4+2]=sbx[r*4+3]=0.f;
+    }
+  }
+  __syncthreads();
+  for (int task=tid; task<36000; task+=1024){
+    int i = task/24, w = task - (task/24)*24;
+    float ax1=sbx[i*4+0], ay1=sbx[i*4+1], ax2=sbx[i*4+2], ay2=sbx[i*4+3];
+    float aa=(ax2-ax1)*(ay2-ay1);
     unsigned long long m = 0ull;
-    if (i < 1500){
-      for (int jj=0; jj<64; ++jj){
-        int j = w*64 + jj;
-        if (j > i && j < 1500){
-          float bx1=sbx[j][0],by1=sbx[j][1],bx2=sbx[j][2],by2=sbx[j][3];
-          float ab=(bx2-bx1)*(by2-by1);
-          float lx=fmaxf(ax1,bx1), ly=fmaxf(ay1,by1);
-          float rx=fminf(ax2,bx2), ry=fminf(ay2,by2);
-          float iw=fmaxf(rx-lx,0.f), ih=fmaxf(ry-ly,0.f);
-          float inter=iw*ih;
-          if (inter/(aa+ab-inter+1e-9f) > 0.7f) m |= (1ull<<jj);
-        }
+    for (int jj=0;jj<64;jj++){
+      int j = w*64 + jj;
+      if (j > i && j < 1500){
+        float bx1=sbx[j*4+0],by1=sbx[j*4+1],bx2=sbx[j*4+2],by2=sbx[j*4+3];
+        float ab=(bx2-bx1)*(by2-by1);
+        float lx=fmaxf(ax1,bx1), ly=fmaxf(ay1,by1);
+        float rx=fminf(ax2,bx2), ry=fminf(ay2,by2);
+        float iw=fmaxf(rx-lx,0.f), ih=fmaxf(ry-ly,0.f);
+        float inter=iw*ih;
+        if (inter/(aa+ab-inter+1e-9f) > 0.7f) m |= (1ull<<jj);
       }
     }
     masks[((size_t)b*1536 + i)*24 + w] = m;
   }
-}
-
-__global__ __launch_bounds__(1024) void nms_scan_final(
-    const unsigned long long* __restrict__ masks, const int* __restrict__ sorder,
-    const float* __restrict__ lvl_boxes, const float* __restrict__ lvl_scores,
-    float* __restrict__ props){
-  int b = blockIdx.x, tid = threadIdx.x;
-  __shared__ unsigned long long cm[128][24];
-  __shared__ volatile unsigned long long keepw[24];
-  __shared__ unsigned char korig[1536];
-  __shared__ unsigned long long keys[2048];
+  __threadfence_block();
+  __syncthreads();
+  unsigned long long* cm = reinterpret_cast<unsigned long long*>(sbx);
   if (tid < 24) keepw[tid] = (tid==23) ? ((1ull<<28)-1ull) : ~0ull;
   for (int c=0; c<12; ++c){
     __syncthreads();
     for (int t=tid; t<128*24; t+=1024)
-      cm[t/24][t%24] = masks[((size_t)b*1536 + c*128)*24 + t];
+      cm[t] = masks[((size_t)b*1536 + c*128)*24 + t];
     __syncthreads();
     if (tid < 24){
-      int lim = (c==11) ? 84 : 128;
+      int lim = (c==11) ? 92 : 128;
       for (int il=0; il<lim; ++il){
         int i = c*128 + il;
         unsigned long long kw = keepw[i>>6];
-        if ((kw>>(i&63)) & 1ull) keepw[tid] &= ~cm[il][tid];
+        if ((kw>>(i&63)) & 1ull) keepw[tid] &= ~cm[il*24+tid];
       }
     }
   }
   __syncthreads();
   for (int r=tid; r<1500; r+=1024){
     unsigned long long kw = keepw[r>>6];
-    korig[sorder[(size_t)b*1536 + r]] = (unsigned char)((kw>>(r&63)) & 1ull);
-  }
-  __syncthreads();
-  const float* ls = lvl_scores + (size_t)b*1500;
-  const float* lb = lvl_boxes + (size_t)b*1500*4;
+    korig[order_[r]] = (unsigned char)((kw>>(r&63)) & 1ull);
+  }
+  __syncthreads();
   for (int i=tid;i<2048;i+=1024){
     if (i<1500){
-      float s = korig[i] ? ls[i] : -1e9f;
-      keys[i] = ((unsigned long long)fkey(s)<<32)|(uint32_t)(~(uint32_t)i);
+      float sv = korig[i] ? ls[i] : -1e9f;
+      keys[i] = ((unsigned long long)fkey(sv)<<32)|(uint32_t)(~(uint32_t)i);
     } else keys[i]=0ull;
   }
   __syncthreads();
@@ -814,26 +848,6 @@
   }
 }
 
-__global__ __launch_bounds__(256) void reduce_splitk(
-    const float* __restrict__ part, const float* __restrict__ bias,
-    float* __restrict__ out, int MN, int Nmask, int relu){
-  int i4 = (blockIdx.x*256 + threadIdx.x)*4;
-  if (i4 < MN){
-    float4 s0 = *reinterpret_cast<const float4*>(&part[i4]);
-    float4 s1 = *reinterpret_cast<const float4*>(&part[(size_t)MN + i4]);
-    float4 s2 = *reinterpret_cast<const float4*>(&part[(size_t)2*MN + i4]);
-    float4 s3 = *reinterpret_cast<const float4*>(&part[(size_t)3*MN + i4]);
-    float4 bb = *reinterpret_cast<const float4*>(&bias[i4 & Nmask]);
-    float4 r;
-    r.x = s0.x+s1.x+s2.x+s3.x+bb.x;
-    r.y = s0.y+s1.y+s2.y+s3.y+bb.y;
-    r.z = s0.z+s1.z+s2.z+s3.z+bb.z;
-    r.w = s0.w+s1.w+s2.w+s3.w+bb.w;
-    if (relu){ r.x=fmaxf(r.x,0.f); r.y=fmaxf(r.y,0.f); r.z=fmaxf(r.z,0.f); r.w=fmaxf(r.w,0.f); }
-    *reinterpret_cast<float4*>(&out[i4]) = r;
-  }
-}
-
 __global__ __launch_bounds__(256) void fc_heads(
     const float* __restrict__ x,
     const float* __restrict__ wcls, const float* __restrict__ bcls,
@@ -985,7 +999,6 @@
 
   float* ws = (float*)d_ws;
   float* featT = ws;
-  float* fc1o  = ws;
   float* fc2o  = ws + 1048576;
   float* clsb  = ws + 2097152;
   float* boxb  = ws + 2099200;
@@ -997,37 +1010,21 @@
   float* dels       = roiX + 7113750;
   float* lvl_boxes  = roiX + 8688750;
   float* lvl_scores = roiX + 8700750;
-  float* nms_snb    = roiX + 8703750;
-  int*   nms_order  = (int*)(roiX + 8716038);
-  unsigned long long* nms_masks = (unsigned long long*)(roiX + 8719110);
-  float* wrp2  = roiX + 8866568;
-  unsigned short* wBh = (unsigned short*)(roiX + 8887048);
-  unsigned short* wBm = (unsigned short*)(roiX + 9181960);
-  unsigned short* wBl = (unsigned short*)(roiX + 9476872);
-  uint32_t* gh1 = (uint32_t*)(roiX + 9771784);
-  uint32_t* gh2 = (uint32_t*)(roiX + 9796360);
-  uint32_t* gh3 = (uint32_t*)(roiX + 9820936);
-  int*      candCnt = (int*)(roiX + 9822472);
-  unsigned long long* cand = (unsigned long long*)(roiX + 9822480);
-
-  prep_all<<<2583, 256, 0, stream>>>(rpn_conv_w, rpn_cls_w, rpn_box_w,
-                                     wBh, wBm, wBl, wrp2, gh1);
-  feat_transpose_all<<<dim3(412,8,2), 256, 0, stream>>>(feat0, feat1, feat2, featT);
-  conv_mfma<<<832, 256, 0, stream>>>(featT, wBh, wBm, wBl, rpn_conv_b, tP);
+  unsigned long long* nms_masks = (unsigned long long*)(roiX + 8703750);
+  float* wrp2  = roiX + 8851206;
+  float* wB    = roiX + 8871686;
+  uint32_t* gh1 = (uint32_t*)(roiX + 9461510);
+
+  prep_tr<<<9072, 256, 0, stream>>>(rpn_conv_w, rpn_cls_w, rpn_box_w,
+                                    wB, wrp2, gh1, feat0, feat1, feat2, featT);
+  conv_mfma<<<832, 256, 0, stream>>>(featT, wB, rpn_conv_b, tP);
   rpn_heads_all<<<dim3(207,2), 256, 0, stream>>>(tP, wrp2, rpn_cls_b, rpn_box_b, objs, dels);
   tk_hist1<<<dim3(8,6), 1024, 0, stream>>>(objs, gh1);
-  tk_hist2<<<dim3(8,6), 1024, 0, stream>>>(objs, gh1, gh2);
-  tk_hist3<<<dim3(8,6), 1024, 0, stream>>>(objs, gh1, gh2, gh3);
-  tk_compact<<<dim3(8,6), 1024, 0, stream>>>(objs, gh1, gh2, gh3, candCnt, cand);
-  tk_sortdecode<<<dim3(3,2), 1024, 0, stream>>>(objs, dels, candCnt, cand, lvl_boxes, lvl_scores);
-  nms_sort<<<2, 1024, 0, stream>>>(lvl_boxes, lvl_scores, nms_snb, nms_order);
-  nms_mask<<<dim3(24,2), 256, 0, stream>>>(nms_snb, nms_masks);
-  nms_scan_final<<<2, 1024, 0, stream>>>(nms_masks, nms_order, lvl_boxes, lvl_scores, props);
+  tk_rest<<<6, 1024, 0, stream>>>(objs, dels, gh1, lvl_boxes, lvl_scores);
+  nms_all<<<2, 1024, 0, stream>>>(lvl_boxes, lvl_scores, nms_masks, props);
   roi_align<<<1024, 256, 0, stream>>>(featT, props, roiX);
   gemm_mfma<<<dim3(16,8,4), 256, 0, stream>>>(roiX, fc1_w, parts, 1024, 1024, 12544, 3136);
-  reduce_splitk<<<1024, 256, 0, stream>>>(parts, fc1_b, fc1o, 1024*1024, 1023, 1);
-  gemm_mfma<<<dim3(16,8,4), 256, 0, stream>>>(fc1o, fc2_w, parts, 1024, 1024, 1024, 256);
-  reduce_splitk<<<1024, 256, 0, stream>>>(parts, fc2_b, fc2o, 1024*1024, 1023, 1);
+  gemm_fc2<<<dim3(16,8), 256, 0, stream>>>(parts, fc1_b, fc2_w, fc2_b, fc2o);
   fc_heads<<<1024, 256, 0, stream>>>(fc2o, cls_w, cls_b, box_w, box_b, clsb, boxb);
   postprocess_kernel<<<2, 1024, 0, stream>>>(clsb, boxb, props, (float*)d_out);
 }
```
